# Kernel optimization log

Hardware: AMD Instinct MI355X
Metric: run time of the kernel (lower is better)

Reference implementation:

```python
import jax, jax.numpy as jnp
import numpy as np

B, G, P, H = 32, 5000, 5000, 64
N = B * G
E_CO, E_GG = 1600000, 100000

def _bn(x, g, b):
    # BatchNorm1d in training mode: biased batch stats, eps=1e-5
    m = x.mean(0); v = x.var(0)
    return g * (x - m) * jax.lax.rsqrt(v + 1e-5) + b

def _renorm(t):
    # nn.Embedding(max_norm=True) -> rows renormed to L2 norm <= 1
    n = jnp.linalg.norm(t, axis=1, keepdims=True)
    return t * jnp.minimum(1.0, 1.0 / jnp.maximum(n, 1e-12))

def _sgconv(x, src, dst, w, W, b):
    # SGConv(K=1): gcn_norm (self-loops w=1, symmetric deg norm) spmm, then Linear
    n = x.shape[0]
    sl = jnp.arange(n)
    s = jnp.concatenate([src, sl]); d = jnp.concatenate([dst, sl])
    ww = jnp.concatenate([w, jnp.ones((n,), x.dtype)])
    deg = jax.ops.segment_sum(ww, d, num_segments=n)
    dinv = jnp.where(deg > 0, jax.lax.rsqrt(deg), 0.0)
    coef = dinv[s] * ww * dinv[d]
    agg = jax.ops.segment_sum(coef[:, None] * x[s], d, num_segments=n)
    return agg @ W.T + b

def _mlp3(x, W, b, g, bt):
    # MLP([h,h,h]): Lin-BN-ReLU-Lin-BN (trailing ReLU stripped by [:-1])
    h = jax.nn.relu(_bn(x @ W[0].T + b[0], g[0], bt[0]))
    return _bn(h @ W[1].T + b[1], g[1], bt[1])

def _gears(x, pert_idx, ei_co, w_co, ei_go, w_go, ei_bg, w_bg,
           gene_tab, pos_tab, go_tab, bg_tab, bn_g, bn_b, sg_W, sg_b,
           mlp_W, mlp_b, mlp_g, mlp_bt,
           rec_W1, rec_b1, rec_g1, rec_bt1, rec_W2, rec_b2, rec_g2, rec_bt2,
           indv_w1, indv_b1,
           cg_W1, cg_b1, cg_g1, cg_bt1, cg_W2, cg_b2, cg_g2, cg_bt2,
           indv_w2, indv_b2):
    nb = pert_idx.shape[0]
    ng = gene_tab.shape[0]
    emb = jnp.tile(_renorm(gene_tab), (nb, 1))                     # [B*G,H]
    base = jax.nn.relu(_bn(emb, bn_g[0], bn_b[0]))                 # bn_emb + emb_trans
    pos = jnp.tile(_renorm(pos_tab), (nb, 1))
    pos = _sgconv(pos, ei_co[0], ei_co[1], w_co, sg_W[0], sg_b[0]) # 1 gene-pos GNN layer, no trailing relu
    base = base + 0.2 * pos
    base = _mlp3(base, mlp_W[1], mlp_b[1], mlp_g[1], mlp_bt[1])    # emb_trans_v2
    pgo = _sgconv(_renorm(go_tab), ei_go[0], ei_go[1], w_go, sg_W[1], sg_b[1])
    pbg = _sgconv(_renorm(bg_tab), ei_bg[0], ei_bg[1], w_bg, sg_W[2], sg_b[2])
    pglob = _mlp3(pgo + pbg, mlp_W[0], mlp_b[0], mlp_g[0], mlp_bt[0])  # pert_emb_comb_trans
    base = base.reshape(nb, ng, -1)
    # one valid pert per graph -> pert_track reduces to a gather; pert_fuse then broadcast-add
    emb_total = _mlp3(pglob[pert_idx], mlp_W[2], mlp_b[2], mlp_g[2], mlp_bt[2])  # [B,H]
    base = base + emb_total[:, None, :]
    base = base.reshape(nb * ng, -1)
    base = jax.nn.relu(_bn(base, bn_g[1], bn_b[1]))                # bn_pert_base + transform
    h = jax.nn.relu(_bn(base @ rec_W1.T + rec_b1, rec_g1, rec_bt1))
    out = _bn(h @ rec_W2.T + rec_b2, rec_g2, rec_bt2).reshape(nb, ng, -1)
    w1 = jnp.einsum('bgh,gh->bg', out, indv_w1) + indv_b1          # per-gene decoder 1
    cg = jax.nn.relu(_bn(w1 @ cg_W1.T + cg_b1, cg_g1, cg_bt1))
    cg = _bn(cg @ cg_W2.T + cg_b2, cg_g2, cg_bt2)                  # cross_gene_state [B,H]
    cat = jnp.concatenate([w1[..., None], jnp.broadcast_to(cg[:, None, :], (nb, ng, cg.shape[-1]))], -1)
    out2 = jnp.einsum('bgk,gk->bg', cat, indv_w2) + indv_b2        # per-gene decoder 2
    return out2 + x.reshape(nb, ng)

def setup_inputs():
    ks = jax.random.split(jax.random.key(0), 48)
    rn = lambda i, sh, s=0.05: jax.random.normal(ks[i], sh, jnp.float32) * s
    return {
        "x": rn(0, (N,), 1.0),
        "pert_idx": jax.random.randint(ks[1], (B,), 0, P),
        "ei_co": jax.random.randint(ks[2], (2, E_CO), 0, N),
        "w_co": jax.random.uniform(ks[3], (E_CO,), jnp.float32),
        "ei_go": jax.random.randint(ks[4], (2, E_GG), 0, P),
        "w_go": jax.random.uniform(ks[5], (E_GG,), jnp.float32),
        "ei_bg": jax.random.randint(ks[6], (2, E_GG), 0, P),
        "w_bg": jax.random.uniform(ks[7], (E_GG,), jnp.float32),
        "gene_tab": rn(8, (G, H), 1.0),
        "pos_tab": rn(9, (G, H), 1.0),
        "go_tab": rn(10, (P, H), 1.0),
        "bg_tab": rn(11, (P, H), 1.0),
        "bn_g": jnp.ones((2, H)), "bn_b": jnp.zeros((2, H)),
        "sg_W": rn(12, (3, H, H)), "sg_b": jnp.zeros((3, H)),
        "mlp_W": rn(13, (3, 2, H, H)), "mlp_b": jnp.zeros((3, 2, H)),
        "mlp_g": jnp.ones((3, 2, H)), "mlp_bt": jnp.zeros((3, 2, H)),
        "rec_W1": rn(14, (2 * H, H)), "rec_b1": jnp.zeros((2 * H,)),
        "rec_g1": jnp.ones((2 * H,)), "rec_bt1": jnp.zeros((2 * H,)),
        "rec_W2": rn(15, (H, 2 * H)), "rec_b2": jnp.zeros((H,)),
        "rec_g2": jnp.ones((H,)), "rec_bt2": jnp.zeros((H,)),
        "indv_w1": rn(16, (G, H)), "indv_b1": rn(17, (G,)),
        "cg_W1": rn(18, (H, G), 0.01), "cg_b1": jnp.zeros((H,)),
        "cg_g1": jnp.ones((H,)), "cg_bt1": jnp.zeros((H,)),
        "cg_W2": rn(19, (H, H)), "cg_b2": jnp.zeros((H,)),
        "cg_g2": jnp.ones((H,)), "cg_bt2": jnp.zeros((H,)),
        "indv_w2": rn(20, (G, H + 1)), "indv_b2": rn(21, (G,)),
    }

def reference(x, pert_idx, ei_co, w_co, ei_go, w_go, ei_bg, w_bg,
              gene_tab, pos_tab, go_tab, bg_tab, bn_g, bn_b, sg_W, sg_b,
              mlp_W, mlp_b, mlp_g, mlp_bt,
              rec_W1, rec_b1, rec_g1, rec_bt1, rec_W2, rec_b2, rec_g2, rec_bt2,
              indv_w1, indv_b1,
              cg_W1, cg_b1, cg_g1, cg_bt1, cg_W2, cg_b2, cg_g2, cg_bt2,
              indv_w2, indv_b2):
    return _gears(x, pert_idx, ei_co, w_co, ei_go, w_go, ei_bg, w_bg,
                  gene_tab, pos_tab, go_tab, bg_tab, bn_g, bn_b, sg_W, sg_b,
                  mlp_W, mlp_b, mlp_g, mlp_bt,
                  rec_W1, rec_b1, rec_g1, rec_bt1, rec_W2, rec_b2, rec_g2, rec_bt2,
                  indv_w1, indv_b1,
                  cg_W1, cg_b1, cg_g1, cg_bt1, cg_W2, cg_b2, cg_g2, cg_bt2,
                  indv_w2, indv_b2)
```

## Files before the change

### kernel.cpp

```cpp
#include <hip/hip_runtime.h>

typedef unsigned int u32;
typedef unsigned short u16;

constexpr int Gn  = 5000;
constexpr int Bn  = 32;
constexpr int Pn  = 5000;
constexpr int Nn  = Bn * Gn;
constexpr int ECO = 1600000;
constexpr int EGG = 100000;
constexpr int NTILES = Nn / 128;
constexpr int PTILES = 40;
constexpr int NBK = 625;
constexpr int EPB2 = ECO / 256;

constexpr int oS2 = 128;
constexpr int oZERO = 1536;
constexpr int oA1 = 2048, oB1 = 2112, oA2 = 2176, oB2 = 2240;
constexpr int oA4 = 2304, oB4 = 2432;
constexpr int oA5 = 2560, oB5 = 2624;
constexpr int oAG = 2688, oBG = 2752;
constexpr int oAP1 = 2816, oBP1 = 2880, oAP2 = 2944, oBP2 = 3008;
constexpr int oAvec = 3072, oCvec = 3136, oCcP = 3200;
constexpr int oM  = 4096, oM1 = 8192;
constexpr int oE2 = 16384, oEMB = 18432, oCGRAW = 20480, oCG2 = 22528;
constexpr int oRG  = 24576;
constexpr int oRP  = oRG  + Gn * 64;
constexpr int oQ   = oRP  + Gn * 64;
constexpr int oRGO = oQ   + Gn * 64;
constexpr int oRBG = oRGO + Pn * 64;
constexpr int oPM  = oRBG + Pn * 64;
constexpr int oABG = oPM + Pn * 64;
constexpr int oM1B = oABG + Pn * 64;
constexpr int oM2B = oM1B + Pn * 64;
constexpr int oDGO = oM2B + Pn * 64;
constexpr int oDBG = oDGO + Pn;
constexpr int oDEG = oDBG + Pn;
constexpr int oW1  = oDEG + Nn;
constexpr int oBUF0 = oW1 + Nn;
constexpr int oBUF1 = oBUF0 + Nn * 64;
constexpr size_t WS_FLOATS = (size_t)oBUF1 + (size_t)Nn * 64;

__device__ inline u16 f2bf(float f) {
  u32 u = __float_as_uint(f);
  u = (u + 0x7fffu + ((u >> 16) & 1u)) >> 16;
  return (u16)u;
}
__device__ inline float bflo(u32 v) { return __uint_as_float(v << 16); }
__device__ inline float bfhi(u32 v) { return __uint_as_float(v & 0xffff0000u); }
__device__ inline float bf2f(u16 v) { return __uint_as_float((u32)v << 16); }

typedef __attribute__((ext_vector_type(8))) short short8v;
typedef __attribute__((ext_vector_type(4))) float f32x4;

__global__ __launch_bounds__(256) void kzero(float* p, int n) {
  int i = blockIdx.x * 256 + threadIdx.x;
  if (i < n) p[i] = 0.f;
}

__global__ __launch_bounds__(256) void krenorm(const float* __restrict__ in, float* __restrict__ out,
                                               float* __restrict__ partial, u16* __restrict__ outb, int rows) {
  int lane = threadIdx.x & 63, wv = threadIdx.x >> 6;
  int gw = blockIdx.x * 4 + wv, nw = gridDim.x * 4;
  float ps = 0.f, pq = 0.f;
  for (int r = gw; r < rows; r += nw) {
    float v = in[r * 64 + lane];
    float sq = v * v;
    for (int off = 32; off; off >>= 1) sq += __shfl_xor(sq, off, 64);
    float nn = sqrtf(sq);
    float s = fminf(1.f, 1.f / fmaxf(nn, 1e-12f));
    float o = v * s;
    out[r * 64 + lane] = o;
    if (outb) outb[r * 64 + lane] = f2bf(o);
    ps += o; pq += o * o;
  }
  if (!partial) return;
  __shared__ float red[4][64], red2[4][64];
  red[wv][lane] = ps; red2[wv][lane] = pq;
  __syncthreads();
  if (wv == 0) {
    float s = red[0][lane] + red[1][lane] + red[2][lane] + red[3][lane];
    float q = red2[0][lane] + red2[1][lane] + red2[2][lane] + red2[3][lane];
    partial[blockIdx.x * 128 + lane] = s;
    partial[blockIdx.x * 128 + 64 + lane] = q;
  }
}

__global__ __launch_bounds__(1024) void kredfin(const float* __restrict__ part, int nblk, int outc,
                                                const float* __restrict__ g, const float* __restrict__ bt,
                                                float* __restrict__ a, float* __restrict__ b,
                                                float* __restrict__ outSQ, float invn) {
  __shared__ float rs[16][64], rq[16][64];
  int t = threadIdx.x, c = t & 63, seg = t >> 6;
  int col = blockIdx.x * 64 + c;
  int pitch = 2 * outc;
  float s = 0.f, q = 0.f;
  for (int r = seg; r < nblk; r += 16) {
    s += part[(size_t)r * pitch + col];
    q += part[(size_t)r * pitch + outc + col];
  }
  rs[seg][c] = s; rq[seg][c] = q;
  __syncthreads();
  if (t < 64) {
    int cc = blockIdx.x * 64 + t;
    float S = 0.f, Q = 0.f;
#pragma unroll
    for (int i = 0; i < 16; i++) { S += rs[i][t]; Q += rq[i][t]; }
    float mean = S * invn;
    float var = Q * invn - mean * mean;
    float sc = g[cc] * rsqrtf(var + 1e-5f);
    a[cc] = sc;
    b[cc] = bt[cc] - mean * sc;
    if (outSQ) { outSQ[cc] = S; outSQ[outc + cc] = Q; }
  }
}

__global__ __launch_bounds__(64) void kredB(const float* __restrict__ part, float* __restrict__ S3B) {
  int b = blockIdx.x;
  int c = threadIdx.x;
  float s = 0.f;
  int r0 = (b == 0) ? 0 : ((b - 1) * Gn) / 128;
  int r1 = ((b + 1) * Gn + 127) / 128;
  if (r1 > NTILES) r1 = NTILES;
  for (int r = r0; r < r1; r++) {
    int bLo = (r * 128) / Gn;
    if (bLo == b) s += part[(size_t)r * 128 + c];
    else if (bLo + 1 == b) s += part[(size_t)r * 128 + 64 + c];
  }
  S3B[b * 64 + c] = s;
}

__global__ __launch_bounds__(256) void ksmallmat(const float* __restrict__ A, const float* __restrict__ Bm,
                                                 float alpha, const float* __restrict__ bias,
                                                 const float* __restrict__ bv1, const float* __restrict__ bv2,
                                                 float beta, float* __restrict__ Mout, int mpitch,
                                                 float* __restrict__ cvec) {
  __shared__ float As[4096], Bs[4096];
  int t = threadIdx.x;
  for (int m = 0; m < 16; m++) { As[m * 256 + t] = A[m * 256 + t]; Bs[m * 256 + t] = Bm[m * 256 + t]; }
  __syncthreads();
  int j = t & 63, ig = t >> 6;
  for (int ii = 0; ii < 16; ii++) {
    int i = ig * 16 + ii;
    float acc = 0.f;
    for (int k = 0; k < 64; k++) acc += As[i * 64 + k] * Bs[k * 64 + j];
    Mout[i * mpitch + j] = alpha * acc;
  }
  if (cvec && t < 64) {
    float acc = bias ? bias[t] : 0.f;
    for (int k = 0; k < 64; k++) {
      float bb = (bv1 ? bv1[k] : 0.f) + (bv2 ? bv2[k] : 0.f);
      acc += beta * As[t * 64 + k] * bb;
    }
    cvec[t] = acc;
  }
}

__global__ __launch_bounds__(256) void khist(const int* __restrict__ dst, int* __restrict__ cnt,
                                             int* __restrict__ ticket, int E) {
  int e = blockIdx.x * 256 + threadIdx.x;
  if (e < E) ticket[e] = atomicAdd(&cnt[dst[e]], 1);
}

__global__ __launch_bounds__(256) void kscan1(const int* __restrict__ cnt, int* __restrict__ bsum, int n) {
  __shared__ int sh[256];
  int b = blockIdx.x, t = threadIdx.x;
  int base = b * 1024 + t * 4;
  int s = 0;
#pragma unroll
  for (int j = 0; j < 4; j++) { int i = base + j; if (i < n) s += cnt[i]; }
  sh[t] = s; __syncthreads();
  for (int d = 128; d; d >>= 1) { if (t < d) sh[t] += sh[t + d]; __syncthreads(); }
  if (t == 0) bsum[b] = sh[0];
}
__global__ __launch_bounds__(256) void kscan2(int* bsum, int nb, int* off_n) {
  __shared__ int sh[256];
  int t = threadIdx.x;
  int v = (t < nb) ? bsum[t] : 0;
  sh[t] = v;
  __syncthreads();
  for (int d = 1; d < 256; d <<= 1) {
    int u = (t >= d) ? sh[t - d] : 0;
    __syncthreads();
    sh[t] += u;
    __syncthreads();
  }
  if (t < nb) bsum[t] = sh[t] - v;
  if (t == nb - 1 && off_n) *off_n = sh[t];
}
__global__ __launch_bounds__(256) void kscan3(int* __restrict__ cnt, const int* __restrict__ bsum, int n) {
  __shared__ int sh[256];
  int b = blockIdx.x, t = threadIdx.x;
  int base = b * 1024 + t * 4;
  int c0 = (base + 0 < n) ? cnt[base + 0] : 0;
  int c1 = (base + 1 < n) ? cnt[base + 1] : 0;
  int c2 = (base + 2 < n) ? cnt[base + 2] : 0;
  int c3 = (base + 3 < n) ? cnt[base + 3] : 0;
  int tot = c0 + c1 + c2 + c3;
  sh[t] = tot; __syncthreads();
  for (int d = 1; d < 256; d <<= 1) {
    int v = (t >= d) ? sh[t - d] : 0;
    __syncthreads();
    sh[t] += v;
    __syncthreads();
  }
  int excl = sh[t] - tot + bsum[b];
  if (base + 0 < n) cnt[base + 0] = excl;
  if (base + 1 < n) cnt[base + 1] = excl + c0;
  if (base + 2 < n) cnt[base + 2] = excl + c0 + c1;
  if (base + 3 < n) cnt[base + 3] = excl + c0 + c1 + c2;
}

__global__ __launch_bounds__(256) void kfillt(const int* __restrict__ src, const int* __restrict__ dst,
                                              const float* __restrict__ w, const int* __restrict__ off,
                                              const int* __restrict__ ticket, float2* __restrict__ pack, int E) {
  int e = blockIdx.x * 256 + threadIdx.x;
  if (e >= E) return;
  int d = dst[e];
  int pos = off[d] + ticket[e];
  pack[pos] = make_float2(w[e], __int_as_float(src[e]));
}

__global__ __launch_bounds__(256) void kdinvrow(const int* __restrict__ off, const float2* __restrict__ pack,
                                                float* __restrict__ dinv, int n) {
  int i = blockIdx.x * 256 + threadIdx.x;
  if (i >= n) return;
  int b0 = off[i], b1 = off[i + 1];
  float s = 1.f;
  for (int j = b0; j < b1; j++) s += pack[j].x;
  dinv[i] = rsqrtf(s);
}

__global__ __launch_bounds__(256) void kpsort(const int* __restrict__ src, const int* __restrict__ dst,
                                              const float* __restrict__ w, float2* __restrict__ stg,
                                              int* __restrict__ Cg, int* __restrict__ Lg) {
  __shared__ int cnt[NBK];
  __shared__ int loff[NBK];
  __shared__ int cur[NBK];
  __shared__ int ssc[256];
  __shared__ float2 sbuf[EPB2];
  int t = threadIdx.x;
  int e0 = blockIdx.x * EPB2;
  for (int i = t; i < NBK; i += 256) cnt[i] = 0;
  __syncthreads();
  for (int e = e0 + t; e < e0 + EPB2; e += 256) atomicAdd(&cnt[dst[e] >> 8], 1);
  __syncthreads();
  int i0 = t * 3;
  int c3[3];
  int s = 0;
#pragma unroll
  for (int j = 0; j < 3; j++) { int i = i0 + j; c3[j] = (i < NBK) ? cnt[i] : 0; s += c3[j]; }
  ssc[t] = s;
  __syncthreads();
  for (int d = 1; d < 256; d <<= 1) {
    int u = (t >= d) ? ssc[t - d] : 0;
    __syncthreads();
    ssc[t] += u;
    __syncthreads();
  }
  int base = ssc[t] - s;
#pragma unroll
  for (int j = 0; j < 3; j++) {
    int i = i0 + j;
    if (i < NBK) { loff[i] = base; cur[i] = base; }
    base += c3[j];
  }
  __syncthreads();
  for (int e = e0 + t; e < e0 + EPB2; e += 256) {
    int d = dst[e];
    int pos = atomicAdd(&cur[d >> 8], 1);
    sbuf[pos] = make_float2(w[e], __int_as_float(src[e] | ((d & 255) << 18)));
  }
  __syncthreads();
  for (int i = t; i < EPB2; i += 256) stg[(size_t)e0 + i] = sbuf[i];
  for (int i = t; i < NBK; i += 256) {
    Cg[blockIdx.x * NBK + i] = cnt[i];
    Lg[blockIdx.x * NBK + i] = loff[i];
  }
}

__global__ __launch_bounds__(256) void ksumT(const int* __restrict__ Cg, int* __restrict__ T) {
  int bk = blockIdx.x * 256 + threadIdx.x;
  if (bk >= NBK) return;
  int s = 0;
  for (int blk = 0; blk < 256; blk++) s += Cg[blk * NBK + bk];
  T[bk] = s;
}

__global__ __launch_bounds__(256) void kpscan(const int* __restrict__ bcnt, int* __restrict__ bbase,
                                              int* __restrict__ offN) {
  __shared__ int sh[256];
  int t = threadIdx.x;
  int i0 = t * 3;
  int c[3];
  int s = 0;
#pragma unroll
  for (int j = 0; j < 3; j++) { int i = i0 + j; c[j] = (i < NBK) ? bcnt[i] : 0; s += c[j]; }
  sh[t] = s;
  __syncthreads();
  for (int d = 1; d < 256; d <<= 1) {
    int u = (t >= d) ? sh[t - d] : 0;
    __syncthreads();
    sh[t] += u;
    __syncthreads();
  }
  int base = sh[t] - s;
#pragma unroll
  for (int j = 0; j < 3; j++) {
    int i = i0 + j;
    if (i < NBK) bbase[i] = base;
    base += c[j];
  }
  if (t == 255) { bbase[NBK] = base; *offN = base; }
}

__global__ __launch_bounds__(256) void kpcsr2(const int* __restrict__ bbase, const int* __restrict__ Cg,
                                              const int* __restrict__ Lg, const float2* __restrict__ stg,
                                              int* __restrict__ off, float2* __restrict__ pack,
                                              float* __restrict__ dinv) {
  constexpr int CAP = 4096;
  __shared__ float2 ebuf[CAP];
  __shared__ int rh[256];
  __shared__ int sc2[256];
  __shared__ float ws[256];
  __shared__ int nEs;
  int bk = blockIdx.x, t = threadIdx.x;
  int myC = Cg[t * NBK + bk];
  int myL = Lg[t * NBK + bk];
  sc2[t] = myC;
  __syncthreads();
  for (int d = 1; d < 256; d <<= 1) {
    int u = (t >= d) ? sc2[t - d] : 0;
    __syncthreads();
    sc2[t] += u;
    __syncthreads();
  }
  int myO = sc2[t] - myC;
  if (t == 255) nEs = sc2[255];
  rh[t] = 0; ws[t] = 0.f;
  __syncthreads();
  int nE = nEs;
  {
    const float2* sp = &stg[(size_t)t * EPB2 + myL];
    for (int i = 0; i < myC; i++) ebuf[myO + i] = sp[i];
  }
  __syncthreads();
  for (int i = t; i < nE; i += 256) {
    float2 p = ebuf[i];
    int r = (__float_as_int(p.y) >> 18) & 255;
    atomicAdd(&rh[r], 1);
    atomicAdd(&ws[r], p.x);
  }
  __syncthreads();
  int cnt = rh[t];
  sc2[t] = cnt;
  __syncthreads();
  for (int d = 1; d < 256; d <<= 1) {
    int u = (t >= d) ? sc2[t - d] : 0;
    __syncthreads();
    sc2[t] += u;
    __syncthreads();
  }
  int gpos = bbase[bk] + sc2[t] - cnt;
  int grow = (bk << 8) + t;
  off[grow] = gpos;
  dinv[grow] = rsqrtf(1.f + ws[t]);
  rh[t] = gpos;
  __syncthreads();
  for (int i = t; i < nE; i += 256) {
    float2 p = ebuf[i];
    int r = (__float_as_int(p.y) >> 18) & 255;
    int pos = atomicAdd(&rh[r], 1);
    pack[pos] = p;
  }
}

__global__ __launch_bounds__(256) void kgather(const int* __restrict__ off, const float2* __restrict__ pack,
                                               const float* __restrict__ dinv, const float* __restrict__ tab,
                                               u16* __restrict__ aggb, int pitch, int coff, int n) {
  int lane = threadIdx.x & 63;
  int wv = blockIdx.x * 4 + (threadIdx.x >> 6);
  int nw = gridDim.x * 4;
  for (int i = wv; i < n; i += nw) {
    int b0 = off[i], b1 = off[i + 1];
    float di = dinv[i];
    float acc = di * tab[(i % Gn) * 64 + lane];
    for (int base = b0; base < b1; base += 64) {
      int m = b1 - base; if (m > 64) m = 64;
      float cj = 0.f; int idxj = 0;
      if (lane < m) {
        float2 p = pack[base + lane];
        int s = __float_as_int(p.y) & 0x3FFFF;
        cj = p.x * dinv[s];
        idxj = (s % Gn) * 64;
      }
      int j = 0;
      for (; j + 1 < m; j += 2) {
        float c0 = __shfl(cj, j, 64);     int i0 = __shfl(idxj, j, 64);
        float c1 = __shfl(cj, j + 1, 64); int i1 = __shfl(idxj, j + 1, 64);
        float t0 = tab[i0 + lane];
        float t1 = tab[i1 + lane];
        acc = fmaf(c0, t0, acc);
        acc = fmaf(c1, t1, acc);
      }
      if (j < m) {
        float c0 = __shfl(cj, j, 64); int i0 = __shfl(idxj, j, 64);
        acc = fmaf(c0, tab[i0 + lane], acc);
      }
    }
    acc *= di;
    aggb[(size_t)i * pitch + coff + lane] = f2bf(acc);
  }
}

__global__ __launch_bounds__(256) void kgt2(const int* __restrict__ off, const float2* __restrict__ pack,
                                            const float* __restrict__ dinv, const uint4* __restrict__ PMB,
                                            const float4* __restrict__ Q4, u16* __restrict__ Ybf,
                                            float* __restrict__ partS) {
  __shared__ float sstat[128];
  int t = threadIdx.x;
  int lane = t & 63, wv = t >> 6;
  int grp = lane >> 3, le = lane & 7;
  for (int idx = t; idx < 128; idx += 256) sstat[idx] = 0.f;
  __syncthreads();
  float sS[8], sQ[8];
#pragma unroll
  for (int j = 0; j < 8; j++) { sS[j] = 0.f; sQ[j] = 0.f; }
  int base0 = (blockIdx.x * 4 + wv) * 8;
  int stride = gridDim.x * 32;
  for (int i0 = base0; i0 < Nn; i0 += stride) {
    int i = i0 + grp;
    int g = i % Gn;
    int b0 = off[i], b1 = off[i + 1];
    float di = dinv[i];
    float acc[8];
    {
      uint4 tv = PMB[g * 8 + le];
      acc[0] = di * bflo(tv.x); acc[1] = di * bfhi(tv.x);
      acc[2] = di * bflo(tv.y); acc[3] = di * bfhi(tv.y);
      acc[4] = di * bflo(tv.z); acc[5] = di * bfhi(tv.z);
      acc[6] = di * bflo(tv.w); acc[7] = di * bfhi(tv.w);
    }
    for (int base = b0; base < b1; base += 8) {
      int m = b1 - base; if (m > 8) m = 8;
      float cj = 0.f; int ix = 0;
      if (le < m) {
        float2 p = pack[base + le];
        int s = __float_as_int(p.y) & 0x3FFFF;
        cj = p.x * dinv[s];
        ix = s % Gn;
      }
#pragma unroll
      for (int e = 0; e < 8; e++) {
        float c = __shfl(cj, grp * 8 + e, 64);
        int x = __shfl(ix, grp * 8 + e, 64);
        if (e < m) {
          uint4 tv = PMB[x * 8 + le];
          acc[0] = fmaf(c, bflo(tv.x), acc[0]);
          acc[1] = fmaf(c, bfhi(tv.x), acc[1]);
          acc[2] = fmaf(c, bflo(tv.y), acc[2]);
          acc[3] = fmaf(c, bfhi(tv.y), acc[3]);
          acc[4] = fmaf(c, bflo(tv.z), acc[4]);
          acc[5] = fmaf(c, bfhi(tv.z), acc[5]);
          acc[6] = fmaf(c, bflo(tv.w), acc[6]);
          acc[7] = fmaf(c, bfhi(tv.w), acc[7]);
        }
      }
    }
    float4 q0 = Q4[g * 16 + le * 2];
    float4 q1 = Q4[g * 16 + le * 2 + 1];
    float v[8];
    v[0] = fmaf(di, acc[0], q0.x); v[1] = fmaf(di, acc[1], q0.y);
    v[2] = fmaf(di, acc[2], q0.z); v[3] = fmaf(di, acc[3], q0.w);
    v[4] = fmaf(di, acc[4], q1.x); v[5] = fmaf(di, acc[5], q1.y);
    v[6] = fmaf(di, acc[6], q1.z); v[7] = fmaf(di, acc[7], q1.w);
#pragma unroll
    for (int j = 0; j < 8; j++) { sS[j] += v[j]; sQ[j] += v[j] * v[j]; }
    uint4 o;
    o.x = (u32)f2bf(v[0]) | ((u32)f2bf(v[1]) << 16);
    o.y = (u32)f2bf(v[2]) | ((u32)f2bf(v[3]) << 16);
    o.z = (u32)f2bf(v[4]) | ((u32)f2bf(v[5]) << 16);
    o.w = (u32)f2bf(v[6]) | ((u32)f2bf(v[7]) << 16);
    *(uint4*)&Ybf[(size_t)i * 64 + le * 8] = o;
  }
#pragma unroll
  for (int j = 0; j < 8; j++) {
    atomicAdd(&sstat[le * 8 + j], sS[j]);
    atomicAdd(&sstat[64 + le * 8 + j], sQ[j]);
  }
  __syncthreads();
  for (int idx = t; idx < 128; idx += 256) partS[(size_t)blockIdx.x * 128 + idx] = sstat[idx];
}

template <int K, int OUTC, bool PRE, bool EB, bool PERG, bool STATS, bool OUTF32, bool STATB>
__global__ __launch_bounds__(256, 3) void mfgemm(
    const u16* __restrict__ Xb, const float* __restrict__ Wg, const float* __restrict__ bias,
    const float* __restrict__ pa, const float* __restrict__ pb,
    const float* __restrict__ perg, u16* __restrict__ Ybf, float* __restrict__ stats,
    float* __restrict__ statB, int rows) {
  constexpr int NT  = OUTC / 16;
  constexpr int KH  = K / 32;
  constexpr int SLK = K / 8;
  constexpr int SLO = OUTC / 8;
  constexpr int XROW = (K > OUTC ? K : OUTC) * 2;
  __shared__ __align__(16) unsigned char xsb[128 * XROW];
  __shared__ __align__(16) unsigned char wsb[OUTC * K * 2];
  __shared__ float sstat[STATS ? 2 * OUTC : 1];
  __shared__ float sstatB[STATB ? 128 : 1];
  int t = threadIdx.x;
  int l = t & 63, w = t >> 6, lrow = l & 15, lk = l >> 4;
  int R0 = blockIdx.x * 128;

  for (int idx = t; idx < OUTC * SLK; idx += 256) {
    int oc = idx / SLK, s8 = idx % SLK;
    const float* wp = &Wg[oc * K + s8 * 8];
    uint4 o;
    o.x = (u32)f2bf(wp[0]) | ((u32)f2bf(wp[1]) << 16);
    o.y = (u32)f2bf(wp[2]) | ((u32)f2bf(wp[3]) << 16);
    o.z = (u32)f2bf(wp[4]) | ((u32)f2bf(wp[5]) << 16);
    o.w = (u32)f2bf(wp[6]) | ((u32)f2bf(wp[7]) << 16);
    *(uint4*)&wsb[oc * (2 * K) + ((s8 * 16) ^ ((oc & 7) << 4))] = o;
  }
  if constexpr (STATS) for (int idx = t; idx < 2 * OUTC; idx += 256) sstat[idx] = 0.f;
  if constexpr (STATB) for (int idx = t; idx < 128; idx += 256) sstatB[idx] = 0.f;

#pragma unroll
  for (int m = 0; m < SLK / 2; m++) {
    int f = m * 256 + t;
    int r = f / SLK, s8 = f % SLK;
    uint4 u = *(const uint4*)&Xb[(size_t)(R0 + r) * K + s8 * 8];
    if constexpr (PRE) {
      int c0 = s8 * 8;
      float4 A0 = *(const float4*)&pa[c0];
      float4 A1 = *(const float4*)&pa[c0 + 4];
      const float* pbb = EB ? &pb[((R0 + r) / Gn) * 64] : pb;
      float4 B0 = *(const float4*)&pbb[c0];
      float4 B1 = *(const float4*)&pbb[c0 + 4];
      float v0 = fmaxf(fmaf(A0.x, bflo(u.x), B0.x), 0.f);
      float v1 = fmaxf(fmaf(A0.y, bfhi(u.x), B0.y), 0.f);
      float v2 = fmaxf(fmaf(A0.z, bflo(u.y), B0.z), 0.f);
      float v3 = fmaxf(fmaf(A0.w, bfhi(u.y), B0.w), 0.f);
      float v4 = fmaxf(fmaf(A1.x, bflo(u.z), B1.x), 0.f);
      float v5 = fmaxf(fmaf(A1.y, bfhi(u.z), B1.y), 0.f);
      float v6 = fmaxf(fmaf(A1.z, bflo(u.w), B1.z), 0.f);
      float v7 = fmaxf(fmaf(A1.w, bfhi(u.w), B1.w), 0.f);
      u.x = (u32)f2bf(v0) | ((u32)f2bf(v1) << 16);
      u.y = (u32)f2bf(v2) | ((u32)f2bf(v3) << 16);
      u.z = (u32)f2bf(v4) | ((u32)f2bf(v5) << 16);
      u.w = (u32)f2bf(v6) | ((u32)f2bf(v7) << 16);
    }
    *(uint4*)&xsb[r * XROW + ((s8 * 16) ^ ((r & 7) << 4))] = u;
  }
  float bcol[NT];
#pragma unroll
  for (int nt = 0; nt < NT; nt++) bcol[nt] = bias[nt * 16 + lrow];
  __syncthreads();

  short8v af[2][KH];
#pragma unroll
  for (int rt = 0; rt < 2; rt++)
#pragma unroll
    for (int h = 0; h < KH; h++) {
      int row = w * 32 + rt * 16 + lrow;
      af[rt][h] = *(const short8v*)&xsb[row * XROW + ((h * 64 + lk * 16) ^ ((row & 7) << 4))];
    }
  f32x4 acc[2][NT];
#pragma unroll
  for (int rt = 0; rt < 2; rt++)
#pragma unroll
    for (int nt = 0; nt < NT; nt++) {
      f32x4 z = {0.f, 0.f, 0.f, 0.f};
      acc[rt][nt] = z;
    }
#pragma unroll
  for (int nt = 0; nt < NT; nt++) {
    int brow = nt * 16 + lrow;
#pragma unroll
    for (int h = 0; h < KH; h++) {
      short8v bfr = *(const short8v*)&wsb[brow * (2 * K) + ((h * 64 + lk * 16) ^ ((brow & 7) << 4))];
      acc[0][nt] = __builtin_amdgcn_mfma_f32_16x16x32_bf16(af[0][h], bfr, acc[0][nt], 0, 0, 0);
      acc[1][nt] = __builtin_amdgcn_mfma_f32_16x16x32_bf16(af[1][h], bfr, acc[1][nt], 0, 0, 0);
    }
  }
  __syncthreads();

  float sS[NT], sQ[NT], sB0[NT], sB1[NT];
#pragma unroll
  for (int nt = 0; nt < NT; nt++) { sS[nt] = 0.f; sQ[nt] = 0.f; sB0[nt] = 0.f; sB1[nt] = 0.f; }
  int hiStart = STATB ? (R0 / Gn + 1) * Gn : 0x7fffffff;
  float* Yf = (float*)Ybf;
#pragma unroll
  for (int rt = 0; rt < 2; rt++) {
#pragma unroll
    for (int r = 0; r < 4; r++) {
      int orow = w * 32 + rt * 16 + lk * 4 + r;
      int grow = R0 + orow;
      bool valid = grow < rows;
      int qoff = 0;
      if constexpr (PERG) qoff = (grow % Gn) * 64;
#pragma unroll
      for (int nt = 0; nt < NT; nt++) {
        float v = acc[rt][nt][r] + bcol[nt];
        if constexpr (PERG) v += perg[qoff + nt * 16 + lrow];
        if (valid) {
          if constexpr (STATS) { sS[nt] += v; sQ[nt] += v * v; }
          if constexpr (STATB) { if (grow >= hiStart) sB1[nt] += v; else sB0[nt] += v; }
        }
        if constexpr (OUTF32) {
          if (valid) Yf[(size_t)grow * OUTC + nt * 16 + lrow] = v;
        } else {
          *(u16*)&xsb[orow * (2 * OUTC) + ((2 * (nt * 16 + lrow)) ^ ((orow & 7) << 4))] = f2bf(v);
        }
      }
    }
  }
  if constexpr (STATS) {
#pragma unroll
    for (int nt = 0; nt < NT; nt++) {
      atomicAdd(&sstat[nt * 16 + lrow], sS[nt]);
      atomicAdd(&sstat[OUTC + nt * 16 + lrow], sQ[nt]);
    }
  }
  if constexpr (STATB) {
#pragma unroll
    for (int nt = 0; nt < NT; nt++) {
      atomicAdd(&sstatB[nt * 16 + lrow], sB0[nt]);
      atomicAdd(&sstatB[64 + nt * 16 + lrow], sB1[nt]);
    }
  }
  __syncthreads();

  if constexpr (!OUTF32) {
#pragma unroll
    for (int m = 0; m < SLO / 2; m++) {
      int f = m * 256 + t;
      int r = f / SLO, c8 = f % SLO;
      uint4 o = *(const uint4*)&xsb[r * (2 * OUTC) + ((16 * c8) ^ ((r & 7) << 4))];
      *(uint4*)&Ybf[(size_t)(R0 + r) * OUTC + c8 * 8] = o;
    }
  }
  if constexpr (STATS)
    for (int idx = t; idx < 2 * OUTC; idx += 256) stats[(size_t)blockIdx.x * 2 * OUTC + idx] = sstat[idx];
  if constexpr (STATB)
    for (int idx = t; idx < 128; idx += 256) statB[(size_t)blockIdx.x * 128 + idx] = sstatB[idx];
}

__global__ __launch_bounds__(256) void kfinS3e2(const float* __restrict__ S2, const float* __restrict__ g,
                                                const float* __restrict__ bt, const float* __restrict__ a2,
                                                const float* __restrict__ b2, const float* __restrict__ emb,
                                                const float* __restrict__ S3B,
                                                float* __restrict__ Avec, float* __restrict__ e2) {
  __shared__ float a3s[64], b3s[64];
  int t = threadIdx.x;
  if (t < 64) {
    float a2c = a2[t], b2c = b2[t];
    float su = 0.f, sxc = 0.f, sc2 = 0.f;
    for (int b = 0; b < Bn; b++) {
      float cb = b2c + emb[b * 64 + t];
      float sb = S3B[b * 64 + t];
      su += cb;
      sxc += cb * sb;
      sc2 += cb * cb;
    }
    float Su = a2c * S2[t] + (float)Gn * su;
    float Sq = a2c * a2c * S2[64 + t] + 2.f * a2c * sxc + (float)Gn * sc2;
    float mean = Su * (1.f / Nn);
    float var = Sq * (1.f / Nn) - mean * mean;
    float sc = g[t] * rsqrtf(var + 1e-5f);
    float sh = bt[t] - mean * sc;
    a3s[t] = sc; b3s[t] = sh;
    Avec[t] = sc * a2c;
  }
  __syncthreads();
  for (int idx = t; idx < 2048; idx += 256) {
    int c = idx & 63;
    e2[idx] = a3s[c] * (b2[c] + emb[idx]) + b3s[c];
  }
}

__global__ __launch_bounds__(256) void k13_kernel(const u16* __restrict__ R2, const float* __restrict__ a5,
                                                  const float* __restrict__ b5, const float* __restrict__ iw1,
                                                  const float* __restrict__ ib1, float* __restrict__ w1out,
                                                  int rows) {
  int t = blockIdx.x * 256 + threadIdx.x;
  int i = t >> 4, j = t & 15;
  if (i >= rows) return;
  int g = i % Gn;
  uint2 u = *(const uint2*)&R2[(size_t)i * 64 + j * 4];
  float rx = bflo(u.x), ry = bfhi(u.x), rz = bflo(u.y), rw = bfhi(u.y);
  float4 a = ((const float4*)a5)[j];
  float4 b = ((const float4*)b5)[j];
  float4 w = ((const float4*)iw1)[g * 16 + j];
  float p = (a.x * rx + b.x) * w.x + (a.y * ry + b.y) * w.y +
            (a.z * rz + b.z) * w.z + (a.w * rw + b.w) * w.w;
  for (int off = 8; off; off >>= 1) p += __shfl_xor(p, off, 64);
  if (j == 0) w1out[i] = p + ib1[g];
}

__global__ __launch_bounds__(256) void kinitcg(const float* __restrict__ cgb1, float* __restrict__ cgraw) {
  int idx = blockIdx.x * 256 + threadIdx.x;
  if (idx < Bn * 64) cgraw[idx] = cgb1[idx & 63];
}

__global__ __launch_bounds__(256) void kcg1s(const float* __restrict__ w1, const float* __restrict__ cgW1,
                                             float* __restrict__ cgraw) {
  __shared__ float w1s[64 * 36];
  __shared__ float cgs[64 * 65];
  int t = threadIdx.x;
  int k0 = blockIdx.x * 64;
  int kmax = Gn - k0; if (kmax > 64) kmax = 64;
  for (int idx = t; idx < 2048; idx += 256) {
    int row = idx >> 6, k = idx & 63;
    w1s[k * 36 + row] = (k < kmax) ? w1[row * Gn + k0 + k] : 0.f;
  }
  for (int idx = t; idx < 4096; idx += 256) {
    int col = idx >> 6, k = idx & 63;
    cgs[k * 65 + col] = (k < kmax) ? cgW1[col * Gn + k0 + k] : 0.f;
  }
  __syncthreads();
  int col = t & 63, rg = t >> 6;
  float acc[8];
#pragma unroll
  for (int i = 0; i < 8; i++) acc[i] = 0.f;
  for (int k = 0; k < 64; k++) {
    float wk = cgs[k * 65 + col];
    const float* wr = &w1s[k * 36 + rg * 8];
    float4 r0 = *(const float4*)wr;
    float4 r1 = *(const float4*)(wr + 4);
    acc[0] = fmaf(r0.x, wk, acc[0]);
    acc[1] = fmaf(r0.y, wk, acc[1]);
    acc[2] = fmaf(r0.z, wk, acc[2]);
    acc[3] = fmaf(r0.w, wk, acc[3]);
    acc[4] = fmaf(r1.x, wk, acc[4]);
    acc[5] = fmaf(r1.y, wk, acc[5]);
    acc[6] = fmaf(r1.z, wk, acc[6]);
    acc[7] = fmaf(r1.w, wk, acc[7]);
  }
#pragma unroll
  for (int i = 0; i < 8; i++) atomicAdd(&cgraw[(rg * 8 + i) * 64 + col], acc[i]);
}

__global__ __launch_bounds__(256) void kcg2(const float* __restrict__ cgraw, const float* __restrict__ g1,
                                            const float* __restrict__ bt1, const float* __restrict__ W2,
                                            const float* __restrict__ b2, const float* __restrict__ g2,
                                            const float* __restrict__ bt2, float* __restrict__ cg2out) {
  int t = threadIdx.x, c = t & 63, bg = t >> 6;
  __shared__ float hmid[2048], sred[4][64], qred[4][64], asc[64], bsh[64];
  float y[8];
  float ps = 0.f, pq = 0.f;
  for (int jb = 0; jb < 8; jb++) {
    int b = bg * 8 + jb;
    float v = cgraw[b * 64 + c];
    y[jb] = v; ps += v; pq += v * v;
  }
  sred[bg][c] = ps; qred[bg][c] = pq;
  __syncthreads();
  if (t < 64) {
    float s = sred[0][t] + sred[1][t] + sred[2][t] + sred[3][t];
    float q = qred[0][t] + qred[1][t] + qred[2][t] + qred[3][t];
    float mean = s * (1.f / 32.f), var = q * (1.f / 32.f) - mean * mean;
    float sc = g1[t] * rsqrtf(var + 1e-5f);
    asc[t] = sc; bsh[t] = bt1[t] - mean * sc;
  }
  __syncthreads();
  for (int jb = 0; jb < 8; jb++) { int b = bg * 8 + jb; hmid[b * 64 + c] = fmaxf(asc[c] * y[jb] + bsh[c], 0.f); }
  __syncthreads();
  ps = 0.f; pq = 0.f;
  for (int jb = 0; jb < 8; jb++) {
    int b = bg * 8 + jb;
    float a = b2[c];
    for (int k = 0; k < 64; k++) a += hmid[b * 64 + k] * W2[c * 64 + k];
    y[jb] = a; ps += a; pq += a * a;
  }
  sred[bg][c] = ps; qred[bg][c] = pq;
  __syncthreads();
  if (t < 64) {
    float s = sred[0][t] + sred[1][t] + sred[2][t] + sred[3][t];
    float q = qred[0][t] + qred[1][t] + qred[2][t] + qred[3][t];
    float mean = s * (1.f / 32.f), var = q * (1.f / 32.f) - mean * mean;
    float sc = g2[t] * rsqrtf(var + 1e-5f);
    asc[t] = sc; bsh[t] = bt2[t] - mean * sc;
  }
  __syncthreads();
  for (int jb = 0; jb < 8; jb++) { int b = bg * 8 + jb; cg2out[b * 64 + c] = asc[c] * y[jb] + bsh[c]; }
}

__global__ __launch_bounds__(256) void kemb(const u16* __restrict__ m2, const float* __restrict__ aP2,
                                            const float* __restrict__ bP2, const int* __restrict__ pidx,
                                            const float* __restrict__ Wm, const float* __restrict__ bv,
                                            const float* __restrict__ gg, const float* __restrict__ btv,
                                            float* __restrict__ emb) {
  int t = threadIdx.x, c = t & 63, bg = t >> 6;
  __shared__ float xin[2048], hmid[2048], sred[4][64], qred[4][64], asc[64], bsh[64];
  for (int idx = t; idx < 2048; idx += 256) {
    int b = idx >> 6, cc = idx & 63;
    xin[idx] = aP2[cc] * bf2f(m2[(size_t)pidx[b] * 64 + cc]) + bP2[cc];
  }
  __syncthreads();
  float y[8];
  float ps = 0.f, pq = 0.f;
  for (int jb = 0; jb < 8; jb++) {
    int b = bg * 8 + jb;
    float a = bv[c];
    for (int k = 0; k < 64; k++) a += xin[b * 64 + k] * Wm[c * 64 + k];
    y[jb] = a; ps += a; pq += a * a;
  }
  sred[bg][c] = ps; qred[bg][c] = pq;
  __syncthreads();
  if (t < 64) {
    float s = sred[0][t] + sred[1][t] + sred[2][t] + sred[3][t];
    float q = qred[0][t] + qred[1][t] + qred[2][t] + qred[3][t];
    float mean = s * (1.f / 32.f), var = q * (1.f / 32.f) - mean * mean;
    float sc = gg[t] * rsqrtf(var + 1e-5f);
    asc[t] = sc; bsh[t] = btv[t] - mean * sc;
  }
  __syncthreads();
  for (int jb = 0; jb < 8; jb++) { int b = bg * 8 + jb; hmid[b * 64 + c] = fmaxf(asc[c] * y[jb] + bsh[c], 0.f); }
  __syncthreads();
  ps = 0.f; pq = 0.f;
  for (int jb = 0; jb < 8; jb++) {
    int b = bg * 8 + jb;
    float a = bv[64 + c];
    for (int k = 0; k < 64; k++) a += hmid[b * 64 + k] * Wm[4096 + c * 64 + k];
    y[jb] = a; ps += a; pq += a * a;
  }
  sred[bg][c] = ps; qred[bg][c] = pq;
  __syncthreads();
  if (t < 64) {
    float s = sred[0][t] + sred[1][t] + sred[2][t] + sred[3][t];
    float q = qred[0][t] + qred[1][t] + qred[2][t] + qred[3][t];
    float mean = s * (1.f / 32.f), var = q * (1.f / 32.f) - mean * mean;
    float sc = gg[64 + t] * rsqrtf(var + 1e-5f);
    asc[t] = sc; bsh[t] = btv[64 + t] - mean * sc;
  }
  __syncthreads();
  for (int jb = 0; jb < 8; jb++) { int b = bg * 8 + jb; emb[b * 64 + c] = asc[c] * y[jb] + bsh[c]; }
}

__global__ __launch_bounds__(256) void kfinal(const float* __restrict__ w1, const float* __restrict__ cg2,
                                              const float* __restrict__ iw2, const float* __restrict__ ib2,
                                              const float* __restrict__ x, float* __restrict__ out) {
  __shared__ float iws[64 * 65], cgs[2048];
  int t = threadIdx.x;
  int g0 = blockIdx.x * 64;
  for (int idx = t; idx < 64 * 65; idx += 256) {
    int gi = g0 * 65 + idx;
    iws[idx] = (gi < Gn * 65) ? iw2[gi] : 0.f;
  }
  for (int idx = t; idx < 2048; idx += 256) cgs[idx] = cg2[idx];
  __syncthreads();
  int gl = t & 63, bg = t >> 6;
  int g = g0 + gl;
  if (g >= Gn) return;
  float bias = ib2[g];
  for (int jb = 0; jb < 8; jb++) {
    int b = bg * 8 + jb;
    float acc = w1[b * Gn + g] * iws[gl * 65] + bias;
    for (int k = 0; k < 64; k++) acc += cgs[b * 64 + k] * iws[gl * 65 + 1 + k];
    out[b * Gn + g] = acc + x[b * Gn + g];
  }
}

extern "C" void kernel_launch(void* const* d_in, const int* in_sizes, int n_in,
                              void* d_out, int out_size, void* d_ws, size_t ws_size,
                              hipStream_t stream) {
  (void)in_sizes; (void)n_in; (void)out_size;
  if (ws_size < WS_FLOATS * sizeof(float)) return;

  const float* x        = (const float*)d_in[0];
  const int*   pert_idx = (const int*)d_in[1];
  const int*   ei_co    = (const int*)d_in[2];
  const float* w_co     = (const float*)d_in[3];
  const int*   ei_go    = (const int*)d_in[4];
  const float* w_go     = (const float*)d_in[5];
  const int*   ei_bg    = (const int*)d_in[6];
  const float* w_bg     = (const float*)d_in[7];
  const float* gene_tab = (const float*)d_in[8];
  const float* pos_tab  = (const float*)d_in[9];
  const float* go_tab   = (const float*)d_in[10];
  const float* bg_tab   = (const float*)d_in[11];
  const float* bn_g     = (const float*)d_in[12];
  const float* bn_b     = (const float*)d_in[13];
  const float* sg_W     = (const float*)d_in[14];
  const float* sg_b     = (const float*)d_in[15];
  const float* mlp_W    = (const float*)d_in[16];
  const float* mlp_b    = (const float*)d_in[17];
  const float* mlp_g    = (const float*)d_in[18];
  const float* mlp_bt   = (const float*)d_in[19];
  const float* rec_W1   = (const float*)d_in[20];
  const float* rec_b1   = (const float*)d_in[21];
  const float* rec_g1   = (const float*)d_in[22];
  const float* rec_bt1  = (const float*)d_in[23];
  const float* rec_W2   = (const float*)d_in[24];
  const float* rec_b2   = (const float*)d_in[25];
  const float* rec_g2   = (const float*)d_in[26];
  const float* rec_bt2  = (const float*)d_in[27];
  const float* indv_w1  = (const float*)d_in[28];
  const float* indv_b1  = (const float*)d_in[29];
  const float* cg_W1    = (const float*)d_in[30];
  const float* cg_b1    = (const float*)d_in[31];
  const float* cg_g1    = (const float*)d_in[32];
  const float* cg_bt1   = (const float*)d_in[33];
  const float* cg_W2    = (const float*)d_in[34];
  const float* cg_b2    = (const float*)d_in[35];
  const float* cg_g2    = (const float*)d_in[36];
  const float* cg_bt2   = (const float*)d_in[37];
  const float* indv_w2  = (const float*)d_in[38];
  const float* indv_b2  = (const float*)d_in[39];

  float* W = (float*)d_ws;
  float* buf0 = W + oBUF0;
  float* buf1 = W + oBUF1;

  int*    co_off    = (int*)(buf1);
  int*    bbase     = (int*)(buf1 + 200000);
  int*    Tbk       = (int*)(buf1 + 202000);
  int*    sbsum     = (int*)(buf1 + 320128);
  float2* co_pack   = (float2*)(buf1 + 400000);
  int*    go_cnt    = (int*)(buf1 + 3700000);
  float2* go_pack   = (float2*)(buf1 + 3720000);
  int*    bg_cnt    = (int*)(buf1 + 4000000);
  float2* bg_pack   = (float2*)(buf1 + 4020000);
  u16*    RPB       = (u16*)(buf1 + 4220000);
  int*    Cg        = (int*)(buf1 + 4500000);
  int*    Lg        = (int*)(buf1 + 4700000);
  int*    go_ticket = (int*)(buf1 + 6200000);
  int*    bg_ticket = (int*)(buf1 + 6400000);
  u16*    pgi       = (u16*)(buf1 + 6600000);
  u16*    RGB       = (u16*)(buf1 + 6800000);
  float2* co_stg    = (float2*)(buf1 + 6963840);

  float* partS = buf1 + 8000000;
  float* partB = buf1 + 8650000;

  kzero<<<8, 256, 0, stream>>>(W, 2048);
  kzero<<<15, 256, 0, stream>>>(buf1 + 6800000 + 160000, 3840);
  kzero<<<15, 256, 0, stream>>>(buf1 + 4220000 + 160000, 3840);
  kzero<<<30, 256, 0, stream>>>(buf1 + 6600000 + 320000, 7680);
  krenorm<<<160, 256, 0, stream>>>(gene_tab, W + oRG, partS, RGB, Gn);
  kredfin<<<1, 1024, 0, stream>>>(partS, 160, 64, bn_g, bn_b, W + oAG, W + oBG, nullptr, 1.f / Gn);
  krenorm<<<160, 256, 0, stream>>>(pos_tab, W + oRP, nullptr, RPB, Gn);
  krenorm<<<160, 256, 0, stream>>>(go_tab, W + oRGO, nullptr, nullptr, Pn);
  krenorm<<<160, 256, 0, stream>>>(bg_tab, W + oRBG, nullptr, nullptr, Pn);
  ksmallmat<<<1, 256, 0, stream>>>(mlp_W + 8192, sg_W, 0.2f, mlp_b + 128, sg_b, nullptr, 0.2f,
                                   W + oM, 64, W + oCvec);
  ksmallmat<<<1, 256, 0, stream>>>(mlp_W, sg_W + 4096, 1.f, nullptr, nullptr, nullptr, 0.f,
                                   W + oM1, 128, nullptr);
  ksmallmat<<<1, 256, 0, stream>>>(mlp_W, sg_W + 8192, 1.f, mlp_b, sg_b + 64, sg_b + 128, 1.f,
                                   W + oM1 + 64, 128, W + oCcP);
  mfgemm<64, 64, true, false, false, false, true, false><<<PTILES, 256, 0, stream>>>(
      RGB, mlp_W + 8192, W + oCvec, W + oAG, W + oBG, nullptr, (u16*)(W + oQ), nullptr, nullptr, Gn);
  mfgemm<64, 64, false, false, false, false, false, false><<<PTILES, 256, 0, stream>>>(
      RPB, W + oM, W + oZERO, nullptr, nullptr, nullptr, (u16*)(W + oPM), nullptr, nullptr, Gn);

  kzero<<<(5001 + 255) / 256, 256, 0, stream>>>((float*)go_cnt, 5001);
  khist<<<(EGG + 255) / 256, 256, 0, stream>>>(ei_go + EGG, go_cnt, go_ticket, EGG);
  kscan1<<<5, 256, 0, stream>>>(go_cnt, sbsum, Pn);
  kscan2<<<1, 256, 0, stream>>>(sbsum, 5, go_cnt + Pn);
  kscan3<<<5, 256, 0, stream>>>(go_cnt, sbsum, Pn);
  kfillt<<<(EGG + 255) / 256, 256, 0, stream>>>(ei_go, ei_go + EGG, w_go, go_cnt, go_ticket, go_pack, EGG);
  kdinvrow<<<(Pn + 255) / 256, 256, 0, stream>>>(go_cnt, go_pack, W + oDGO, Pn);
  kgather<<<512, 256, 0, stream>>>(go_cnt, go_pack, W + oDGO, W + oRGO, pgi, 128, 0, Pn);

  kzero<<<(5001 + 255) / 256, 256, 0, stream>>>((float*)bg_cnt, 5001);
  khist<<<(EGG + 255) / 256, 256, 0, stream>>>(ei_bg + EGG, bg_cnt, bg_ticket, EGG);
  kscan1<<<5, 256, 0, stream>>>(bg_cnt, sbsum, Pn);
  kscan2<<<1, 256, 0, stream>>>(sbsum, 5, bg_cnt + Pn);
  kscan3<<<5, 256, 0, stream>>>(bg_cnt, sbsum, Pn);
  kfillt<<<(EGG + 255) / 256, 256, 0, stream>>>(ei_bg, ei_bg + EGG, w_bg, bg_cnt, bg_ticket, bg_pack, EGG);
  kdinvrow<<<(Pn + 255) / 256, 256, 0, stream>>>(bg_cnt, bg_pack, W + oDBG, Pn);
  kgather<<<512, 256, 0, stream>>>(bg_cnt, bg_pack, W + oDBG, W + oRBG, pgi, 128, 64, Pn);

  mfgemm<128, 64, false, false, false, true, false, false><<<PTILES, 256, 0, stream>>>(
      pgi, W + oM1, W + oCcP, nullptr, nullptr, nullptr, (u16*)(W + oM1B), partS, nullptr, Pn);
  kredfin<<<1, 1024, 0, stream>>>(partS, PTILES, 64, mlp_g, mlp_bt, W + oAP1, W + oBP1, nullptr, 1.f / Pn);
  mfgemm<64, 64, true, false, false, true, false, false><<<PTILES, 256, 0, stream>>>(
      (u16*)(W + oM1B), mlp_W + 4096, mlp_b + 64, W + oAP1, W + oBP1, nullptr,
      (u16*)(W + oM2B), partS, nullptr, Pn);
  kredfin<<<1, 1024, 0, stream>>>(partS, PTILES, 64, mlp_g + 64, mlp_bt + 64, W + oAP2, W + oBP2, nullptr, 1.f / Pn);
  kemb<<<1, 256, 0, stream>>>((u16*)(W + oM2B), W + oAP2, W + oBP2, pert_idx,
                              mlp_W + 16384, mlp_b + 256, mlp_g + 256, mlp_bt + 256, W + oEMB);

  kpsort<<<256, 256, 0, stream>>>(ei_co, ei_co + ECO, w_co, co_stg, Cg, Lg);
  ksumT<<<3, 256, 0, stream>>>(Cg, Tbk);
  kpscan<<<1, 256, 0, stream>>>(Tbk, bbase, co_off + Nn);
  kpcsr2<<<NBK, 256, 0, stream>>>(bbase, Cg, Lg, co_stg, co_off, co_pack, W + oDEG);

  kgt2<<<2048, 256, 0, stream>>>(co_off, co_pack, W + oDEG, (const uint4*)(W + oPM),
                                 (const float4*)(W + oQ), (u16*)buf0, partS);
  kredfin<<<1, 1024, 0, stream>>>(partS, 2048, 64, mlp_g + 128, mlp_bt + 128, W + oA1, W + oB1, nullptr, 1.f / Nn);

  mfgemm<64, 64, true, false, false, true, false, true><<<NTILES, 256, 0, stream>>>(
      (const u16*)buf0, mlp_W + 12288, mlp_b + 192, W + oA1, W + oB1, nullptr,
      (u16*)buf1, partS, partB, Nn);
  kredfin<<<1, 1024, 0, stream>>>(partS, NTILES, 64, mlp_g + 192, mlp_bt + 192, W + oA2, W + oB2, W + oS2, 1.f / Nn);
  kredB<<<32, 64, 0, stream>>>(partB, W + oE2);
  kfinS3e2<<<1, 256, 0, stream>>>(W + oS2, bn_g + 64, bn_b + 64, W + oA2, W + oB2, W + oEMB,
                                  W + oE2, W + oAvec, W + oE2);
  mfgemm<64, 128, true, true, false, true, false, false><<<NTILES, 256, 0, stream>>>(
      (const u16*)buf1, rec_W1, rec_b1, W + oAvec, W + oE2, nullptr, (u16*)buf0, partS, nullptr, Nn);
  kredfin<<<2, 1024, 0, stream>>>(partS, NTILES, 128, rec_g1, rec_bt1, W + oA4, W + oB4, nullptr, 1.f / Nn);
  mfgemm<128, 64, true, false, false, true, false, false><<<NTILES, 256, 0, stream>>>(
      (const u16*)buf0, rec_W2, rec_b2, W + oA4, W + oB4, nullptr, (u16*)buf1, partS, nullptr, Nn);
  kredfin<<<1, 1024, 0, stream>>>(partS, NTILES, 64, rec_g2, rec_bt2, W + oA5, W + oB5, nullptr, 1.f / Nn);
  k13_kernel<<<(Nn * 16 + 255) / 256, 256, 0, stream>>>((const u16*)buf1, W + oA5, W + oB5, indv_w1, indv_b1,
                                                        W + oW1, Nn);
  kinitcg<<<8, 256, 0, stream>>>(cg_b1, W + oCGRAW);
  kcg1s<<<(Gn + 63) / 64, 256, 0, stream>>>(W + oW1, cg_W1, W + oCGRAW);
  kcg2<<<1, 256, 0, stream>>>(W + oCGRAW, cg_g1, cg_bt1, cg_W2, cg_b2, cg_g2, cg_bt2, W + oCG2);
  kfinal<<<(Gn + 63) / 64, 256, 0, stream>>>(W + oW1, W + oCG2, indv_w2, indv_b2, x, (float*)d_out);
}
```

Baseline: 751.0 us.

## Merge small setup kernels and process two rows per group in gather

Several small kernels are merged into multi-segment launches: the zero fills, the four table renorms, and the GO and BG graph CSR build steps (histogram, scan, fill, dinv, gather). Each merged kernel picks its input set from the block index. This cuts the number of launches and lets the two independent small graphs run at the same time. The co-expression gather kernel kgt2 is replaced by kgt3, which interleaves two rows (A and B) per lane group so more independent loads are in flight. The cost is higher register pressure and more branch divergence inside the merged kernels.

```diff
diff --git a/kernel.cpp b/kernel.cpp
--- a/kernel.cpp
+++ b/kernel.cpp
@@ -13,6 +13,7 @@
 constexpr int PTILES = 40;
 constexpr int NBK = 625;
 constexpr int EPB2 = ECO / 256;
+constexpr int NBE = (EGG + 255) / 256;
 
 constexpr int oS2 = 128;
 constexpr int oZERO = 1536;
@@ -53,17 +54,33 @@
 typedef __attribute__((ext_vector_type(8))) short short8v;
 typedef __attribute__((ext_vector_type(4))) float f32x4;
 
-__global__ __launch_bounds__(256) void kzero(float* p, int n) {
+__global__ __launch_bounds__(256) void kzero4(float* p0, int n0, float* p1, int n1,
+                                              float* p2, int n2, float* p3, int n3) {
   int i = blockIdx.x * 256 + threadIdx.x;
-  if (i < n) p[i] = 0.f;
-}
-
-__global__ __launch_bounds__(256) void krenorm(const float* __restrict__ in, float* __restrict__ out,
-                                               float* __restrict__ partial, u16* __restrict__ outb, int rows) {
-  int lane = threadIdx.x & 63, wv = threadIdx.x >> 6;
-  int gw = blockIdx.x * 4 + wv, nw = gridDim.x * 4;
+  if (i < n0) p0[i] = 0.f;
+  if (i < n1) p1[i] = 0.f;
+  if (i < n2) p2[i] = 0.f;
+  if (i < n3) p3[i] = 0.f;
+}
+__global__ __launch_bounds__(256) void kzero2(int* a, int* b, int n) {
+  int i = blockIdx.x * 256 + threadIdx.x;
+  if (i < n) { a[i] = 0; b[i] = 0; }
+}
+
+__global__ __launch_bounds__(256) void krenorm4(const float* __restrict__ in0, const float* __restrict__ in1,
+                                                const float* __restrict__ in2, const float* __restrict__ in3,
+                                                float* __restrict__ o0, float* __restrict__ o1,
+                                                float* __restrict__ o2, float* __restrict__ o3,
+                                                u16* __restrict__ ob0, u16* __restrict__ ob1,
+                                                float* __restrict__ partial) {
+  int seg = blockIdx.x / 160, blk = blockIdx.x % 160;
+  const float* in = seg == 0 ? in0 : seg == 1 ? in1 : seg == 2 ? in2 : in3;
+  float* out = seg == 0 ? o0 : seg == 1 ? o1 : seg == 2 ? o2 : o3;
+  u16* outb = seg == 0 ? ob0 : seg == 1 ? ob1 : nullptr;
+  int lane = threadIdx.x & 63, wvv = threadIdx.x >> 6;
+  int gw = blk * 4 + wvv, nw = 640;
   float ps = 0.f, pq = 0.f;
-  for (int r = gw; r < rows; r += nw) {
+  for (int r = gw; r < 5000; r += nw) {
     float v = in[r * 64 + lane];
     float sq = v * v;
     for (int off = 32; off; off >>= 1) sq += __shfl_xor(sq, off, 64);
@@ -74,15 +91,15 @@
     if (outb) outb[r * 64 + lane] = f2bf(o);
     ps += o; pq += o * o;
   }
-  if (!partial) return;
+  if (seg != 0) return;
   __shared__ float red[4][64], red2[4][64];
-  red[wv][lane] = ps; red2[wv][lane] = pq;
-  __syncthreads();
-  if (wv == 0) {
+  red[wvv][lane] = ps; red2[wvv][lane] = pq;
+  __syncthreads();
+  if (wvv == 0) {
     float s = red[0][lane] + red[1][lane] + red[2][lane] + red[3][lane];
     float q = red2[0][lane] + red2[1][lane] + red2[2][lane] + red2[3][lane];
-    partial[blockIdx.x * 128 + lane] = s;
-    partial[blockIdx.x * 128 + 64 + lane] = q;
+    partial[blk * 128 + lane] = s;
+    partial[blk * 128 + 64 + lane] = q;
   }
 }
 
@@ -156,15 +173,26 @@
   }
 }
 
-__global__ __launch_bounds__(256) void khist(const int* __restrict__ dst, int* __restrict__ cnt,
-                                             int* __restrict__ ticket, int E) {
-  int e = blockIdx.x * 256 + threadIdx.x;
-  if (e < E) ticket[e] = atomicAdd(&cnt[dst[e]], 1);
-}
-
-__global__ __launch_bounds__(256) void kscan1(const int* __restrict__ cnt, int* __restrict__ bsum, int n) {
+__global__ __launch_bounds__(256) void khist2(const int* __restrict__ dA, int* __restrict__ cA, int* __restrict__ tA,
+                                              const int* __restrict__ dB, int* __restrict__ cB, int* __restrict__ tB,
+                                              int E, int nbe) {
+  int sel = blockIdx.x >= nbe;
+  int blk = sel ? blockIdx.x - nbe : blockIdx.x;
+  const int* dst = sel ? dB : dA;
+  int* cnt = sel ? cB : cA;
+  int* tick = sel ? tB : tA;
+  int e = blk * 256 + threadIdx.x;
+  if (e < E) tick[e] = atomicAdd(&cnt[dst[e]], 1);
+}
+
+__global__ __launch_bounds__(256) void kscan1m(const int* __restrict__ cA, const int* __restrict__ cB,
+                                               int* __restrict__ bsA, int* __restrict__ bsB, int n, int nblk) {
   __shared__ int sh[256];
-  int b = blockIdx.x, t = threadIdx.x;
+  int sel = blockIdx.x >= nblk;
+  int b = sel ? blockIdx.x - nblk : blockIdx.x;
+  const int* cnt = sel ? cB : cA;
+  int* bsum = sel ? bsB : bsA;
+  int t = threadIdx.x;
   int base = b * 1024 + t * 4;
   int s = 0;
 #pragma unroll
@@ -173,24 +201,35 @@
   for (int d = 128; d; d >>= 1) { if (t < d) sh[t] += sh[t + d]; __syncthreads(); }
   if (t == 0) bsum[b] = sh[0];
 }
-__global__ __launch_bounds__(256) void kscan2(int* bsum, int nb, int* off_n) {
+
+__global__ __launch_bounds__(256) void kscan2m(int* __restrict__ bsA, int* __restrict__ bsB, int nb,
+                                               int* __restrict__ totA, int* __restrict__ totB) {
   __shared__ int sh[256];
   int t = threadIdx.x;
-  int v = (t < nb) ? bsum[t] : 0;
+  int sel = t >> 7, lt = t & 127;
+  int* bsum = sel ? bsB : bsA;
+  int v = (lt < nb) ? bsum[lt] : 0;
   sh[t] = v;
   __syncthreads();
-  for (int d = 1; d < 256; d <<= 1) {
-    int u = (t >= d) ? sh[t - d] : 0;
+  for (int d = 1; d < 128; d <<= 1) {
+    int u = (lt >= d) ? sh[t - d] : 0;
     __syncthreads();
     sh[t] += u;
     __syncthreads();
   }
-  if (t < nb) bsum[t] = sh[t] - v;
-  if (t == nb - 1 && off_n) *off_n = sh[t];
-}
-__global__ __launch_bounds__(256) void kscan3(int* __restrict__ cnt, const int* __restrict__ bsum, int n) {
+  if (lt < nb) bsum[lt] = sh[t] - v;
+  if (lt == nb - 1) *(sel ? totB : totA) = sh[t];
+}
+
+__global__ __launch_bounds__(256) void kscan3m(int* __restrict__ cA, int* __restrict__ cB,
+                                               const int* __restrict__ bsA, const int* __restrict__ bsB,
+                                               int n, int nblk) {
   __shared__ int sh[256];
-  int b = blockIdx.x, t = threadIdx.x;
+  int sel = blockIdx.x >= nblk;
+  int b = sel ? blockIdx.x - nblk : blockIdx.x;
+  int* cnt = sel ? cB : cA;
+  const int* bsum = sel ? bsB : bsA;
+  int t = threadIdx.x;
   int base = b * 1024 + t * 4;
   int c0 = (base + 0 < n) ? cnt[base + 0] : 0;
   int c1 = (base + 1 < n) ? cnt[base + 1] : 0;
@@ -211,19 +250,37 @@
   if (base + 3 < n) cnt[base + 3] = excl + c0 + c1 + c2;
 }
 
-__global__ __launch_bounds__(256) void kfillt(const int* __restrict__ src, const int* __restrict__ dst,
-                                              const float* __restrict__ w, const int* __restrict__ off,
-                                              const int* __restrict__ ticket, float2* __restrict__ pack, int E) {
-  int e = blockIdx.x * 256 + threadIdx.x;
+__global__ __launch_bounds__(256) void kfilltm(const int* __restrict__ sA, const int* __restrict__ dA,
+                                               const float* __restrict__ wA, const int* __restrict__ oA,
+                                               const int* __restrict__ tA, float2* __restrict__ pA,
+                                               const int* __restrict__ sB, const int* __restrict__ dB,
+                                               const float* __restrict__ wB, const int* __restrict__ oB,
+                                               const int* __restrict__ tB, float2* __restrict__ pB,
+                                               int E, int nbe) {
+  int sel = blockIdx.x >= nbe;
+  int blk = sel ? blockIdx.x - nbe : blockIdx.x;
+  const int* src = sel ? sB : sA;
+  const int* dst = sel ? dB : dA;
+  const float* w = sel ? wB : wA;
+  const int* off = sel ? oB : oA;
+  const int* tick = sel ? tB : tA;
+  float2* pack = sel ? pB : pA;
+  int e = blk * 256 + threadIdx.x;
   if (e >= E) return;
   int d = dst[e];
-  int pos = off[d] + ticket[e];
-  pack[pos] = make_float2(w[e], __int_as_float(src[e]));
-}
-
-__global__ __launch_bounds__(256) void kdinvrow(const int* __restrict__ off, const float2* __restrict__ pack,
-                                                float* __restrict__ dinv, int n) {
-  int i = blockIdx.x * 256 + threadIdx.x;
+  pack[off[d] + tick[e]] = make_float2(w[e], __int_as_float(src[e]));
+}
+
+__global__ __launch_bounds__(256) void kdinvrowm(const int* __restrict__ oA, const float2* __restrict__ pA,
+                                                 float* __restrict__ vA, const int* __restrict__ oB,
+                                                 const float2* __restrict__ pB, float* __restrict__ vB,
+                                                 int n, int nbe) {
+  int sel = blockIdx.x >= nbe;
+  int blk = sel ? blockIdx.x - nbe : blockIdx.x;
+  const int* off = sel ? oB : oA;
+  const float2* pack = sel ? pB : pA;
+  float* dinv = sel ? vB : vA;
+  int i = blk * 256 + threadIdx.x;
   if (i >= n) return;
   int b0 = off[i], b1 = off[i + 1];
   float s = 1.f;
@@ -231,157 +288,22 @@
   dinv[i] = rsqrtf(s);
 }
 
-__global__ __launch_bounds__(256) void kpsort(const int* __restrict__ src, const int* __restrict__ dst,
-                                              const float* __restrict__ w, float2* __restrict__ stg,
-                                              int* __restrict__ Cg, int* __restrict__ Lg) {
-  __shared__ int cnt[NBK];
-  __shared__ int loff[NBK];
-  __shared__ int cur[NBK];
-  __shared__ int ssc[256];
-  __shared__ float2 sbuf[EPB2];
-  int t = threadIdx.x;
-  int e0 = blockIdx.x * EPB2;
-  for (int i = t; i < NBK; i += 256) cnt[i] = 0;
-  __syncthreads();
-  for (int e = e0 + t; e < e0 + EPB2; e += 256) atomicAdd(&cnt[dst[e] >> 8], 1);
-  __syncthreads();
-  int i0 = t * 3;
-  int c3[3];
-  int s = 0;
-#pragma unroll
-  for (int j = 0; j < 3; j++) { int i = i0 + j; c3[j] = (i < NBK) ? cnt[i] : 0; s += c3[j]; }
-  ssc[t] = s;
-  __syncthreads();
-  for (int d = 1; d < 256; d <<= 1) {
-    int u = (t >= d) ? ssc[t - d] : 0;
-    __syncthreads();
-    ssc[t] += u;
-    __syncthreads();
-  }
-  int base = ssc[t] - s;
-#pragma unroll
-  for (int j = 0; j < 3; j++) {
-    int i = i0 + j;
-    if (i < NBK) { loff[i] = base; cur[i] = base; }
-    base += c3[j];
-  }
-  __syncthreads();
-  for (int e = e0 + t; e < e0 + EPB2; e += 256) {
-    int d = dst[e];
-    int pos = atomicAdd(&cur[d >> 8], 1);
-    sbuf[pos] = make_float2(w[e], __int_as_float(src[e] | ((d & 255) << 18)));
-  }
-  __syncthreads();
-  for (int i = t; i < EPB2; i += 256) stg[(size_t)e0 + i] = sbuf[i];
-  for (int i = t; i < NBK; i += 256) {
-    Cg[blockIdx.x * NBK + i] = cnt[i];
-    Lg[blockIdx.x * NBK + i] = loff[i];
-  }
-}
-
-__global__ __launch_bounds__(256) void ksumT(const int* __restrict__ Cg, int* __restrict__ T) {
-  int bk = blockIdx.x * 256 + threadIdx.x;
-  if (bk >= NBK) return;
-  int s = 0;
-  for (int blk = 0; blk < 256; blk++) s += Cg[blk * NBK + bk];
-  T[bk] = s;
-}
-
-__global__ __launch_bounds__(256) void kpscan(const int* __restrict__ bcnt, int* __restrict__ bbase,
-                                              int* __restrict__ offN) {
-  __shared__ int sh[256];
-  int t = threadIdx.x;
-  int i0 = t * 3;
-  int c[3];
-  int s = 0;
-#pragma unroll
-  for (int j = 0; j < 3; j++) { int i = i0 + j; c[j] = (i < NBK) ? bcnt[i] : 0; s += c[j]; }
-  sh[t] = s;
-  __syncthreads();
-  for (int d = 1; d < 256; d <<= 1) {
-    int u = (t >= d) ? sh[t - d] : 0;
-    __syncthreads();
-    sh[t] += u;
-    __syncthreads();
-  }
-  int base = sh[t] - s;
-#pragma unroll
-  for (int j = 0; j < 3; j++) {
-    int i = i0 + j;
-    if (i < NBK) bbase[i] = base;
-    base += c[j];
-  }
-  if (t == 255) { bbase[NBK] = base; *offN = base; }
-}
-
-__global__ __launch_bounds__(256) void kpcsr2(const int* __restrict__ bbase, const int* __restrict__ Cg,
-                                              const int* __restrict__ Lg, const float2* __restrict__ stg,
-                                              int* __restrict__ off, float2* __restrict__ pack,
-                                              float* __restrict__ dinv) {
-  constexpr int CAP = 4096;
-  __shared__ float2 ebuf[CAP];
-  __shared__ int rh[256];
-  __shared__ int sc2[256];
-  __shared__ float ws[256];
-  __shared__ int nEs;
-  int bk = blockIdx.x, t = threadIdx.x;
-  int myC = Cg[t * NBK + bk];
-  int myL = Lg[t * NBK + bk];
-  sc2[t] = myC;
-  __syncthreads();
-  for (int d = 1; d < 256; d <<= 1) {
-    int u = (t >= d) ? sc2[t - d] : 0;
-    __syncthreads();
-    sc2[t] += u;
-    __syncthreads();
-  }
-  int myO = sc2[t] - myC;
-  if (t == 255) nEs = sc2[255];
-  rh[t] = 0; ws[t] = 0.f;
-  __syncthreads();
-  int nE = nEs;
-  {
-    const float2* sp = &stg[(size_t)t * EPB2 + myL];
-    for (int i = 0; i < myC; i++) ebuf[myO + i] = sp[i];
-  }
-  __syncthreads();
-  for (int i = t; i < nE; i += 256) {
-    float2 p = ebuf[i];
-    int r = (__float_as_int(p.y) >> 18) & 255;
-    atomicAdd(&rh[r], 1);
-    atomicAdd(&ws[r], p.x);
-  }
-  __syncthreads();
-  int cnt = rh[t];
-  sc2[t] = cnt;
-  __syncthreads();
-  for (int d = 1; d < 256; d <<= 1) {
-    int u = (t >= d) ? sc2[t - d] : 0;
-    __syncthreads();
-    sc2[t] += u;
-    __syncthreads();
-  }
-  int gpos = bbase[bk] + sc2[t] - cnt;
-  int grow = (bk << 8) + t;
-  off[grow] = gpos;
-  dinv[grow] = rsqrtf(1.f + ws[t]);
-  rh[t] = gpos;
-  __syncthreads();
-  for (int i = t; i < nE; i += 256) {
-    float2 p = ebuf[i];
-    int r = (__float_as_int(p.y) >> 18) & 255;
-    int pos = atomicAdd(&rh[r], 1);
-    pack[pos] = p;
-  }
-}
-
-__global__ __launch_bounds__(256) void kgather(const int* __restrict__ off, const float2* __restrict__ pack,
-                                               const float* __restrict__ dinv, const float* __restrict__ tab,
-                                               u16* __restrict__ aggb, int pitch, int coff, int n) {
+__global__ __launch_bounds__(256) void kgatherm(const int* __restrict__ oA, const float2* __restrict__ pA,
+                                                const float* __restrict__ vA, const float* __restrict__ tA,
+                                                const int* __restrict__ oB, const float2* __restrict__ pB,
+                                                const float* __restrict__ vB, const float* __restrict__ tB,
+                                                u16* __restrict__ aggb, int n, int halfBlocks) {
+  int sel = blockIdx.x >= halfBlocks;
+  int blk = sel ? blockIdx.x - halfBlocks : blockIdx.x;
+  const int* off = sel ? oB : oA;
+  const float2* pack = sel ? pB : pA;
+  const float* dinv = sel ? vB : vA;
+  const float* tab = sel ? tB : tA;
+  int coff = sel ? 64 : 0;
   int lane = threadIdx.x & 63;
-  int wv = blockIdx.x * 4 + (threadIdx.x >> 6);
-  int nw = gridDim.x * 4;
-  for (int i = wv; i < n; i += nw) {
+  int wvv = blk * 4 + (threadIdx.x >> 6);
+  int nw = halfBlocks * 4;
+  for (int i = wvv; i < n; i += nw) {
     int b0 = off[i], b1 = off[i + 1];
     float di = dinv[i];
     float acc = di * tab[(i % Gn) * 64 + lane];
@@ -409,79 +331,260 @@
       }
     }
     acc *= di;
-    aggb[(size_t)i * pitch + coff + lane] = f2bf(acc);
-  }
-}
-
-__global__ __launch_bounds__(256) void kgt2(const int* __restrict__ off, const float2* __restrict__ pack,
+    aggb[(size_t)i * 128 + coff + lane] = f2bf(acc);
+  }
+}
+
+__global__ __launch_bounds__(256) void kpsort(const int* __restrict__ src, const int* __restrict__ dst,
+                                              const float* __restrict__ w, float2* __restrict__ stg,
+                                              int* __restrict__ Cg, int* __restrict__ Lg) {
+  __shared__ int cnt[NBK];
+  __shared__ int loff[NBK];
+  __shared__ int cur[NBK];
+  __shared__ int ssc[256];
+  __shared__ float2 sbuf[EPB2];
+  int t = threadIdx.x;
+  int e0 = blockIdx.x * EPB2;
+  for (int i = t; i < NBK; i += 256) cnt[i] = 0;
+  __syncthreads();
+  for (int e = e0 + t; e < e0 + EPB2; e += 256) atomicAdd(&cnt[dst[e] >> 8], 1);
+  __syncthreads();
+  int i0 = t * 3;
+  int c3[3];
+  int s = 0;
+#pragma unroll
+  for (int j = 0; j < 3; j++) { int i = i0 + j; c3[j] = (i < NBK) ? cnt[i] : 0; s += c3[j]; }
+  ssc[t] = s;
+  __syncthreads();
+  for (int d = 1; d < 256; d <<= 1) {
+    int u = (t >= d) ? ssc[t - d] : 0;
+    __syncthreads();
+    ssc[t] += u;
+    __syncthreads();
+  }
+  int base = ssc[t] - s;
+#pragma unroll
+  for (int j = 0; j < 3; j++) {
+    int i = i0 + j;
+    if (i < NBK) { loff[i] = base; cur[i] = base; }
+    base += c3[j];
+  }
+  __syncthreads();
+  for (int e = e0 + t; e < e0 + EPB2; e += 256) {
+    int d = dst[e];
+    int pos = atomicAdd(&cur[d >> 8], 1);
+    sbuf[pos] = make_float2(w[e], __int_as_float(src[e] | ((d & 255) << 18)));
+  }
+  __syncthreads();
+  for (int i = t; i < EPB2; i += 256) stg[(size_t)e0 + i] = sbuf[i];
+  for (int i = t; i < NBK; i += 256) {
+    Cg[blockIdx.x * NBK + i] = cnt[i];
+    Lg[blockIdx.x * NBK + i] = loff[i];
+  }
+}
+
+__global__ __launch_bounds__(256) void ksumT(const int* __restrict__ Cg, int* __restrict__ T) {
+  int bk = blockIdx.x * 256 + threadIdx.x;
+  if (bk >= NBK) return;
+  int s = 0;
+  for (int blk = 0; blk < 256; blk++) s += Cg[blk * NBK + bk];
+  T[bk] = s;
+}
+
+__global__ __launch_bounds__(256) void kpscan(const int* __restrict__ bcnt, int* __restrict__ bbase,
+                                              int* __restrict__ offN) {
+  __shared__ int sh[256];
+  int t = threadIdx.x;
+  int i0 = t * 3;
+  int c[3];
+  int s = 0;
+#pragma unroll
+  for (int j = 0; j < 3; j++) { int i = i0 + j; c[j] = (i < NBK) ? bcnt[i] : 0; s += c[j]; }
+  sh[t] = s;
+  __syncthreads();
+  for (int d = 1; d < 256; d <<= 1) {
+    int u = (t >= d) ? sh[t - d] : 0;
+    __syncthreads();
+    sh[t] += u;
+    __syncthreads();
+  }
+  int base = sh[t] - s;
+#pragma unroll
+  for (int j = 0; j < 3; j++) {
+    int i = i0 + j;
+    if (i < NBK) bbase[i] = base;
+    base += c[j];
+  }
+  if (t == 255) { bbase[NBK] = base; *offN = base; }
+}
+
+__global__ __launch_bounds__(256) void kpcsr2(const int* __restrict__ bbase, const int* __restrict__ Cg,
+                                              const int* __restrict__ Lg, const float2* __restrict__ stg,
+                                              int* __restrict__ off, float2* __restrict__ pack,
+                                              float* __restrict__ dinv) {
+  constexpr int CAP = 4096;
+  __shared__ float2 ebuf[CAP];
+  __shared__ int rh[256];
+  __shared__ int sc2[256];
+  __shared__ float ws[256];
+  __shared__ int nEs;
+  int bk = blockIdx.x, t = threadIdx.x;
+  int myC = Cg[t * NBK + bk];
+  int myL = Lg[t * NBK + bk];
+  sc2[t] = myC;
+  __syncthreads();
+  for (int d = 1; d < 256; d <<= 1) {
+    int u = (t >= d) ? sc2[t - d] : 0;
+    __syncthreads();
+    sc2[t] += u;
+    __syncthreads();
+  }
+  int myO = sc2[t] - myC;
+  if (t == 255) nEs = sc2[255];
+  rh[t] = 0; ws[t] = 0.f;
+  __syncthreads();
+  int nE = nEs;
+  {
+    const float2* sp = &stg[(size_t)t * EPB2 + myL];
+    for (int i = 0; i < myC; i++) ebuf[myO + i] = sp[i];
+  }
+  __syncthreads();
+  for (int i = t; i < nE; i += 256) {
+    float2 p = ebuf[i];
+    int r = (__float_as_int(p.y) >> 18) & 255;
+    atomicAdd(&rh[r], 1);
+    atomicAdd(&ws[r], p.x);
+  }
+  __syncthreads();
+  int cnt = rh[t];
+  sc2[t] = cnt;
+  __syncthreads();
+  for (int d = 1; d < 256; d <<= 1) {
+    int u = (t >= d) ? sc2[t - d] : 0;
+    __syncthreads();
+    sc2[t] += u;
+    __syncthreads();
+  }
+  int gpos = bbase[bk] + sc2[t] - cnt;
+  int grow = (bk << 8) + t;
+  off[grow] = gpos;
+  dinv[grow] = rsqrtf(1.f + ws[t]);
+  rh[t] = gpos;
+  __syncthreads();
+  for (int i = t; i < nE; i += 256) {
+    float2 p = ebuf[i];
+    int r = (__float_as_int(p.y) >> 18) & 255;
+    int pos = atomicAdd(&rh[r], 1);
+    pack[pos] = p;
+  }
+}
+
+__global__ __launch_bounds__(256) void kgt3(const int* __restrict__ off, const float2* __restrict__ pack,
                                             const float* __restrict__ dinv, const uint4* __restrict__ PMB,
                                             const float4* __restrict__ Q4, u16* __restrict__ Ybf,
                                             float* __restrict__ partS) {
   __shared__ float sstat[128];
   int t = threadIdx.x;
-  int lane = t & 63, wv = t >> 6;
+  int lane = t & 63, wvv = t >> 6;
   int grp = lane >> 3, le = lane & 7;
   for (int idx = t; idx < 128; idx += 256) sstat[idx] = 0.f;
   __syncthreads();
   float sS[8], sQ[8];
 #pragma unroll
   for (int j = 0; j < 8; j++) { sS[j] = 0.f; sQ[j] = 0.f; }
-  int base0 = (blockIdx.x * 4 + wv) * 8;
-  int stride = gridDim.x * 32;
+  int base0 = (blockIdx.x * 4 + wvv) * 16;
+  int stride = gridDim.x * 64;
   for (int i0 = base0; i0 < Nn; i0 += stride) {
-    int i = i0 + grp;
-    int g = i % Gn;
-    int b0 = off[i], b1 = off[i + 1];
-    float di = dinv[i];
-    float acc[8];
+    int iA = i0 + grp, iB = i0 + 8 + grp;
+    int gA = iA % Gn, gB = iB % Gn;
+    int a0 = off[iA], a1 = off[iA + 1];
+    int b0 = off[iB], b1 = off[iB + 1];
+    float diA = dinv[iA], diB = dinv[iB];
+    float accA[8], accB[8];
     {
-      uint4 tv = PMB[g * 8 + le];
-      acc[0] = di * bflo(tv.x); acc[1] = di * bfhi(tv.x);
-      acc[2] = di * bflo(tv.y); acc[3] = di * bfhi(tv.y);
-      acc[4] = di * bflo(tv.z); acc[5] = di * bfhi(tv.z);
-      acc[6] = di * bflo(tv.w); acc[7] = di * bfhi(tv.w);
-    }
-    for (int base = b0; base < b1; base += 8) {
-      int m = b1 - base; if (m > 8) m = 8;
-      float cj = 0.f; int ix = 0;
-      if (le < m) {
-        float2 p = pack[base + le];
+      uint4 tA = PMB[gA * 8 + le];
+      uint4 tB = PMB[gB * 8 + le];
+      accA[0] = diA * bflo(tA.x); accA[1] = diA * bfhi(tA.x);
+      accA[2] = diA * bflo(tA.y); accA[3] = diA * bfhi(tA.y);
+      accA[4] = diA * bflo(tA.z); accA[5] = diA * bfhi(tA.z);
+      accA[6] = diA * bflo(tA.w); accA[7] = diA * bfhi(tA.w);
+      accB[0] = diB * bflo(tB.x); accB[1] = diB * bfhi(tB.x);
+      accB[2] = diB * bflo(tB.y); accB[3] = diB * bfhi(tB.y);
+      accB[4] = diB * bflo(tB.z); accB[5] = diB * bfhi(tB.z);
+      accB[6] = diB * bflo(tB.w); accB[7] = diB * bfhi(tB.w);
+    }
+    int curA = a0, curB = b0;
+    while (curA < a1 || curB < b1) {
+      int mA = a1 - curA; mA = mA > 8 ? 8 : (mA < 0 ? 0 : mA);
+      int mB = b1 - curB; mB = mB > 8 ? 8 : (mB < 0 ? 0 : mB);
+      float cjA = 0.f, cjB = 0.f; int ixA = 0, ixB = 0;
+      if (le < mA) {
+        float2 p = pack[curA + le];
         int s = __float_as_int(p.y) & 0x3FFFF;
-        cj = p.x * dinv[s];
-        ix = s % Gn;
+        cjA = p.x * dinv[s];
+        ixA = s % Gn;
       }
+      if (le < mB) {
+        float2 p = pack[curB + le];
+        int s = __float_as_int(p.y) & 0x3FFFF;
+        cjB = p.x * dinv[s];
+        ixB = s % Gn;
+      }
 #pragma unroll
       for (int e = 0; e < 8; e++) {
-        float c = __shfl(cj, grp * 8 + e, 64);
-        int x = __shfl(ix, grp * 8 + e, 64);
-        if (e < m) {
-          uint4 tv = PMB[x * 8 + le];
-          acc[0] = fmaf(c, bflo(tv.x), acc[0]);
-          acc[1] = fmaf(c, bfhi(tv.x), acc[1]);
-          acc[2] = fmaf(c, bflo(tv.y), acc[2]);
-          acc[3] = fmaf(c, bfhi(tv.y), acc[3]);
-          acc[4] = fmaf(c, bflo(tv.z), acc[4]);
-          acc[5] = fmaf(c, bfhi(tv.z), acc[5]);
-          acc[6] = fmaf(c, bflo(tv.w), acc[6]);
-          acc[7] = fmaf(c, bfhi(tv.w), acc[7]);
+        float cA = __shfl(cjA, grp * 8 + e, 64); int xA = __shfl(ixA, grp * 8 + e, 64);
+        float cB = __shfl(cjB, grp * 8 + e, 64); int xB = __shfl(ixB, grp * 8 + e, 64);
+        if (e < mA) {
+          uint4 tv = PMB[xA * 8 + le];
+          accA[0] = fmaf(cA, bflo(tv.x), accA[0]); accA[1] = fmaf(cA, bfhi(tv.x), accA[1]);
+          accA[2] = fmaf(cA, bflo(tv.y), accA[2]); accA[3] = fmaf(cA, bfhi(tv.y), accA[3]);
+          accA[4] = fmaf(cA, bflo(tv.z), accA[4]); accA[5] = fmaf(cA, bfhi(tv.z), accA[5]);
+          accA[6] = fmaf(cA, bflo(tv.w), accA[6]); accA[7] = fmaf(cA, bfhi(tv.w), accA[7]);
+        }
+        if (e < mB) {
+          uint4 tv = PMB[xB * 8 + le];
+          accB[0] = fmaf(cB, bflo(tv.x), accB[0]); accB[1] = fmaf(cB, bfhi(tv.x), accB[1]);
+          accB[2] = fmaf(cB, bflo(tv.y), accB[2]); accB[3] = fmaf(cB, bfhi(tv.y), accB[3]);
+          accB[4] = fmaf(cB, bflo(tv.z), accB[4]); accB[5] = fmaf(cB, bfhi(tv.z), accB[5]);
+          accB[6] = fmaf(cB, bflo(tv.w), accB[6]); accB[7] = fmaf(cB, bfhi(tv.w), accB[7]);
         }
       }
-    }
-    float4 q0 = Q4[g * 16 + le * 2];
-    float4 q1 = Q4[g * 16 + le * 2 + 1];
-    float v[8];
-    v[0] = fmaf(di, acc[0], q0.x); v[1] = fmaf(di, acc[1], q0.y);
-    v[2] = fmaf(di, acc[2], q0.z); v[3] = fmaf(di, acc[3], q0.w);
-    v[4] = fmaf(di, acc[4], q1.x); v[5] = fmaf(di, acc[5], q1.y);
-    v[6] = fmaf(di, acc[6], q1.z); v[7] = fmaf(di, acc[7], q1.w);
-#pragma unroll
-    for (int j = 0; j < 8; j++) { sS[j] += v[j]; sQ[j] += v[j] * v[j]; }
-    uint4 o;
-    o.x = (u32)f2bf(v[0]) | ((u32)f2bf(v[1]) << 16);
-    o.y = (u32)f2bf(v[2]) | ((u32)f2bf(v[3]) << 16);
-    o.z = (u32)f2bf(v[4]) | ((u32)f2bf(v[5]) << 16);
-    o.w = (u32)f2bf(v[6]) | ((u32)f2bf(v[7]) << 16);
-    *(uint4*)&Ybf[(size_t)i * 64 + le * 8] = o;
+      curA += mA; curB += mB;
+    }
+    {
+      float4 q0 = Q4[gA * 16 + le * 2];
+      float4 q1 = Q4[gA * 16 + le * 2 + 1];
+      float v[8];
+      v[0] = fmaf(diA, accA[0], q0.x); v[1] = fmaf(diA, accA[1], q0.y);
+      v[2] = fmaf(diA, accA[2], q0.z); v[3] = fmaf(diA, accA[3], q0.w);
+      v[4] = fmaf(diA, accA[4], q1.x); v[5] = fmaf(diA, accA[5], q1.y);
+      v[6] = fmaf(diA, accA[6], q1.z); v[7] = fmaf(diA, accA[7], q1.w);
+#pragma unroll
+      for (int j = 0; j < 8; j++) { sS[j] += v[j]; sQ[j] += v[j] * v[j]; }
+      uint4 o;
+      o.x = (u32)f2bf(v[0]) | ((u32)f2bf(v[1]) << 16);
+      o.y = (u32)f2bf(v[2]) | ((u32)f2bf(v[3]) << 16);
+      o.z = (u32)f2bf(v[4]) | ((u32)f2bf(v[5]) << 16);
+      o.w = (u32)f2bf(v[6]) | ((u32)f2bf(v[7]) << 16);
+      *(uint4*)&Ybf[(size_t)iA * 64 + le * 8] = o;
+    }
+    {
+      float4 q0 = Q4[gB * 16 + le * 2];
+      float4 q1 = Q4[gB * 16 + le * 2 + 1];
+      float v[8];
+      v[0] = fmaf(diB, accB[0], q0.x); v[1] = fmaf(diB, accB[1], q0.y);
+      v[2] = fmaf(diB, accB[2], q0.z); v[3] = fmaf(diB, accB[3], q0.w);
+      v[4] = fmaf(diB, accB[4], q1.x); v[5] = fmaf(diB, accB[5], q1.y);
+      v[6] = fmaf(diB, accB[6], q1.z); v[7] = fmaf(diB, accB[7], q1.w);
+#pragma unroll
+      for (int j = 0; j < 8; j++) { sS[j] += v[j]; sQ[j] += v[j] * v[j]; }
+      uint4 o;
+      o.x = (u32)f2bf(v[0]) | ((u32)f2bf(v[1]) << 16);
+      o.y = (u32)f2bf(v[2]) | ((u32)f2bf(v[3]) << 16);
+      o.z = (u32)f2bf(v[4]) | ((u32)f2bf(v[5]) << 16);
+      o.w = (u32)f2bf(v[6]) | ((u32)f2bf(v[7]) << 16);
+      *(uint4*)&Ybf[(size_t)iB * 64 + le * 8] = o;
+    }
   }
 #pragma unroll
   for (int j = 0; j < 8; j++) {
@@ -933,15 +1036,14 @@
   float* partS = buf1 + 8000000;
   float* partB = buf1 + 8650000;
 
-  kzero<<<8, 256, 0, stream>>>(W, 2048);
-  kzero<<<15, 256, 0, stream>>>(buf1 + 6800000 + 160000, 3840);
-  kzero<<<15, 256, 0, stream>>>(buf1 + 4220000 + 160000, 3840);
-  kzero<<<30, 256, 0, stream>>>(buf1 + 6600000 + 320000, 7680);
-  krenorm<<<160, 256, 0, stream>>>(gene_tab, W + oRG, partS, RGB, Gn);
+  kzero4<<<30, 256, 0, stream>>>(W, 2048,
+                                 buf1 + 6800000 + 160000, 3840,
+                                 buf1 + 4220000 + 160000, 3840,
+                                 buf1 + 6600000 + 320000, 7680);
+  krenorm4<<<640, 256, 0, stream>>>(gene_tab, pos_tab, go_tab, bg_tab,
+                                    W + oRG, W + oRP, W + oRGO, W + oRBG,
+                                    RGB, RPB, partS);
   kredfin<<<1, 1024, 0, stream>>>(partS, 160, 64, bn_g, bn_b, W + oAG, W + oBG, nullptr, 1.f / Gn);
-  krenorm<<<160, 256, 0, stream>>>(pos_tab, W + oRP, nullptr, RPB, Gn);
-  krenorm<<<160, 256, 0, stream>>>(go_tab, W + oRGO, nullptr, nullptr, Pn);
-  krenorm<<<160, 256, 0, stream>>>(bg_tab, W + oRBG, nullptr, nullptr, Pn);
   ksmallmat<<<1, 256, 0, stream>>>(mlp_W + 8192, sg_W, 0.2f, mlp_b + 128, sg_b, nullptr, 0.2f,
                                    W + oM, 64, W + oCvec);
   ksmallmat<<<1, 256, 0, stream>>>(mlp_W, sg_W + 4096, 1.f, nullptr, nullptr, nullptr, 0.f,
@@ -953,23 +1055,17 @@
   mfgemm<64, 64, false, false, false, false, false, false><<<PTILES, 256, 0, stream>>>(
       RPB, W + oM, W + oZERO, nullptr, nullptr, nullptr, (u16*)(W + oPM), nullptr, nullptr, Gn);
 
-  kzero<<<(5001 + 255) / 256, 256, 0, stream>>>((float*)go_cnt, 5001);
-  khist<<<(EGG + 255) / 256, 256, 0, stream>>>(ei_go + EGG, go_cnt, go_ticket, EGG);
-  kscan1<<<5, 256, 0, stream>>>(go_cnt, sbsum, Pn);
-  kscan2<<<1, 256, 0, stream>>>(sbsum, 5, go_cnt + Pn);
-  kscan3<<<5, 256, 0, stream>>>(go_cnt, sbsum, Pn);
-  kfillt<<<(EGG + 255) / 256, 256, 0, stream>>>(ei_go, ei_go + EGG, w_go, go_cnt, go_ticket, go_pack, EGG);
-  kdinvrow<<<(Pn + 255) / 256, 256, 0, stream>>>(go_cnt, go_pack, W + oDGO, Pn);
-  kgather<<<512, 256, 0, stream>>>(go_cnt, go_pack, W + oDGO, W + oRGO, pgi, 128, 0, Pn);
-
-  kzero<<<(5001 + 255) / 256, 256, 0, stream>>>((float*)bg_cnt, 5001);
-  khist<<<(EGG + 255) / 256, 256, 0, stream>>>(ei_bg + EGG, bg_cnt, bg_ticket, EGG);
-  kscan1<<<5, 256, 0, stream>>>(bg_cnt, sbsum, Pn);
-  kscan2<<<1, 256, 0, stream>>>(sbsum, 5, bg_cnt + Pn);
-  kscan3<<<5, 256, 0, stream>>>(bg_cnt, sbsum, Pn);
-  kfillt<<<(EGG + 255) / 256, 256, 0, stream>>>(ei_bg, ei_bg + EGG, w_bg, bg_cnt, bg_ticket, bg_pack, EGG);
-  kdinvrow<<<(Pn + 255) / 256, 256, 0, stream>>>(bg_cnt, bg_pack, W + oDBG, Pn);
-  kgather<<<512, 256, 0, stream>>>(bg_cnt, bg_pack, W + oDBG, W + oRBG, pgi, 128, 64, Pn);
+  kzero2<<<20, 256, 0, stream>>>(go_cnt, bg_cnt, 5001);
+  khist2<<<2 * NBE, 256, 0, stream>>>(ei_go + EGG, go_cnt, go_ticket,
+                                      ei_bg + EGG, bg_cnt, bg_ticket, EGG, NBE);
+  kscan1m<<<10, 256, 0, stream>>>(go_cnt, bg_cnt, sbsum, sbsum + 64, Pn, 5);
+  kscan2m<<<1, 256, 0, stream>>>(sbsum, sbsum + 64, 5, go_cnt + Pn, bg_cnt + Pn);
+  kscan3m<<<10, 256, 0, stream>>>(go_cnt, bg_cnt, sbsum, sbsum + 64, Pn, 5);
+  kfilltm<<<2 * NBE, 256, 0, stream>>>(ei_go, ei_go + EGG, w_go, go_cnt, go_ticket, go_pack,
+                                       ei_bg, ei_bg + EGG, w_bg, bg_cnt, bg_ticket, bg_pack, EGG, NBE);
+  kdinvrowm<<<40, 256, 0, stream>>>(go_cnt, go_pack, W + oDGO, bg_cnt, bg_pack, W + oDBG, Pn, 20);
+  kgatherm<<<1024, 256, 0, stream>>>(go_cnt, go_pack, W + oDGO, W + oRGO,
+                                     bg_cnt, bg_pack, W + oDBG, W + oRBG, pgi, Pn, 512);
 
   mfgemm<128, 64, false, false, false, true, false, false><<<PTILES, 256, 0, stream>>>(
       pgi, W + oM1, W + oCcP, nullptr, nullptr, nullptr, (u16*)(W + oM1B), partS, nullptr, Pn);
@@ -986,7 +1082,7 @@
   kpscan<<<1, 256, 0, stream>>>(Tbk, bbase, co_off + Nn);
   kpcsr2<<<NBK, 256, 0, stream>>>(bbase, Cg, Lg, co_stg, co_off, co_pack, W + oDEG);
 
-  kgt2<<<2048, 256, 0, stream>>>(co_off, co_pack, W + oDEG, (const uint4*)(W + oPM),
+  kgt3<<<2048, 256, 0, stream>>>(co_off, co_pack, W + oDEG, (const uint4*)(W + oPM),
                                  (const float4*)(W + oQ), (u16*)buf0, partS);
   kredfin<<<1, 1024, 0, stream>>>(partS, 2048, 64, mlp_g + 128, mlp_bt + 128, W + oA1, W + oB1, nullptr, 1.f / Nn);
 
```

Measured after the change: 705.0 us. -6.1%, faster.
